# Kernel tuning notes

Measured on AMD Instinct MI355X. Metric: run time of the kernel, lower is better.

Reference implementation:

```python
import jax, jax.numpy as jnp
import numpy as np

IN_DIM, OUT_DIM = 256, 10
N_EXPERTS, N_MEM, STEPS, N_SUB, MAX_K = 12, 32, 6, 5, 5
EXPERT_DIMS = [2048, 2560, 3072, 3584, 4096, 2304, 2816, 3328, 3840, 4608, 3072, 4096]
MAX_E = 4608
N_ITEMS = 4096
SCALE = IN_DIM ** -0.5

def _gelu(x):
    return jax.nn.gelu(x, approximate=False)

_ACTS = [jax.nn.silu, _gelu, lambda x: x * jnp.tanh(jax.nn.softplus(x)), jax.nn.relu,
         jax.nn.selu, jnp.tanh, jax.nn.softplus, jax.nn.elu]
EXPERT_ACTS = [_ACTS[i % 8] for i in range(N_EXPERTS)]

def _ln(x, s, b, eps=1e-5):
    mu = jnp.mean(x, -1, keepdims=True)
    var = jnp.mean((x - mu) ** 2, -1, keepdims=True)
    return (x - mu) * jax.lax.rsqrt(var + eps) * s + b

def _cell(x, ln_s, ln_b, w1, b1, w2, b2):
    h = _gelu(_ln(x, ln_s, ln_b) @ w1.T + b1)
    return x + h @ w2.T + b2

def _ctx_attn(cur, bank, qw, kw, vw):
    # bank: [n, t, d]; single-query dot attention over a small bank
    q = cur @ qw.T
    k = bank @ kw.T
    v = bank @ vw.T
    attn = jax.nn.softmax(jnp.einsum('nd,ntd->nt', q, k) * SCALE, axis=-1)
    return jnp.einsum('nt,ntd->nd', attn, v)

def _renorm_sparse_topk(probs, active_k):
    tv, ti = jax.lax.top_k(probs, MAX_K)
    mask = (jnp.arange(MAX_K)[None, :] < active_k[:, None]).astype(probs.dtype)
    vals = tv * mask
    rows = jnp.arange(probs.shape[0])[:, None]
    sparse = jnp.zeros_like(probs).at[rows, ti].set(vals)
    return sparse / jnp.maximum(jnp.sum(sparse, -1, keepdims=True), 1e-6)

def _fwd(x, W, b,
         shared_up_w, shared_down_w, shared_ln_s, shared_ln_b, shared_scale,
         mem_keys, mem_vals, mem_q_w, mem_out_w, mem_wg_w, mem_wg_b, mem_wv_w, mem_wv_b,
         depth_q_w, depth_k_w, depth_v_w, depth_out_w,
         rc_ln_s, rc_ln_b, rc_w1, rc_b1, rc_w2, rc_b2,
         ssm_in_w, ssm_out_w, ssm_decay,
         sub_w, sub_b, gate_w, gate_b,
         budget_w, budget_b,
         exp_up, exp_down, exp_ln_s, exp_ln_b,
         halt_w, halt_b,
         aux_up_w, aux_down_w, aux_ln_s, aux_ln_b, aux_gate_w, aux_gate_b,
         rf_ln_s, rf_ln_b, rf_w1, rf_b1, rf_w2, rf_b2, reflect_out_w,
         coll_q_w, coll_k_w, coll_v_w, coll_out_w,
         revisit_w, revisit_b,
         vc_ln_s, vc_ln_b, vc_w1, vc_b1, vc_w2, vc_b2,
         ver_q_w, ver_k_w, ver_v_w, ver_out_w, ver_gate_w, ver_gate_b, correction_out_w,
         mix):
    n = x.shape[0]
    base = x @ W.T + b                                                    # [n, out]
    shared = _ln(jax.nn.silu(x @ shared_up_w.T) @ shared_down_w.T, shared_ln_s, shared_ln_b)
    aux = _ln(_gelu(x @ aux_up_w.T) @ aux_down_w.T, aux_ln_s, aux_ln_b)

    mem_vals_b = jnp.broadcast_to(mem_vals[None], (n, N_MEM, IN_DIM))     # per-item memory
    current = x
    mem_logits = jnp.zeros_like(base)
    depth_logits = jnp.zeros_like(base)
    cum_halt = jnp.zeros((n, 1), x.dtype)
    bank = []
    for s in range(STEPS):
        # memory read
        q = current @ mem_q_w.T
        attn = jax.nn.softmax((q @ mem_keys.T) * SCALE, axis=-1)          # [n, slots]
        mem_read = jnp.einsum('ns,nsd->nd', attn, mem_vals_b)
        # gated memory write
        wg = jax.nn.sigmoid(jnp.concatenate([current, mem_read], -1) @ mem_wg_w.T + mem_wg_b)
        wv = current @ mem_wv_w.T + mem_wv_b
        mem_vals_b = mem_vals_b * (1.0 - wg[..., None]) + wg[..., None] * wv[:, None, :]
        # depth attention over previous states
        if bank:
            depth_ctx = _ctx_attn(current, jnp.stack(bank, 1), depth_q_w, depth_k_w, depth_v_w)
        else:
            depth_ctx = jnp.zeros_like(current)
        current = _cell(current + mem_read + depth_ctx,
                        rc_ln_s[s], rc_ln_b[s], rc_w1[s], rc_b1[s], rc_w2[s], rc_b2[s])
        # SSM adapter (single-step gated state update, residual)
        h = jnp.tanh(current @ ssm_in_w.T) * jax.nn.sigmoid(ssm_decay)
        current = current + h @ ssm_out_w.T
        bank.append(current)
        # halting-weighted contributions
        halt = jax.nn.sigmoid((current @ halt_w[s])[:, None] + halt_b[s])
        w_step = (1.0 - cum_halt) * halt
        mem_logits = mem_logits + w_step * (mem_read @ mem_out_w.T)
        depth_logits = depth_logits + w_step * (depth_ctx @ depth_out_w.T)
        cum_halt = jnp.minimum(cum_halt + halt, 1.0)

    # mixture-of-routers + budgeted sparse top-k
    sub_logits = jnp.einsum('nd,sed->nse', current, sub_w) + sub_b        # [n, sub, exp]
    sub_probs = jax.nn.softmax(sub_logits, axis=-1)
    gate = jax.nn.softmax(current @ gate_w.T + gate_b, axis=-1)           # [n, sub]
    probs = jnp.einsum('ns,nse->ne', gate, sub_probs)
    active_k = jnp.argmax(current @ budget_w.T + budget_b, axis=-1) + 1   # 1..MAX_K
    sparse = _renorm_sparse_topk(probs, active_k)                         # [n, exp]

    expert_out = jnp.zeros_like(base)
    for i in range(N_EXPERTS):
        h = EXPERT_ACTS[i](current @ exp_up[i].T)                         # padded to MAX_E
        o = _ln(h @ exp_down[i].T, exp_ln_s[i], exp_ln_b[i])
        expert_out = expert_out + sparse[:, i:i + 1] * o

    # reflection branch
    r = current
    for i in range(3):
        r = _cell(r, rf_ln_s[i], rf_ln_b[i], rf_w1[i], rf_b1[i], rf_w2[i], rf_b2[i])
    reflect_logits = r @ reflect_out_w.T

    # collective attention over state bank + revisit gate
    stack = jnp.stack(bank, 1)
    coll_ctx = _ctx_attn(current, stack, coll_q_w, coll_k_w, coll_v_w)
    coll_logits = coll_ctx @ coll_out_w.T
    revisit = jax.nn.sigmoid(jnp.concatenate([x, current, coll_ctx], -1) @ revisit_w.T + revisit_b)

    # verifier + correction branch
    v = current
    for i in range(2):
        v = _cell(v, vc_ln_s[i], vc_ln_b[i], vc_w1[i], vc_b1[i], vc_w2[i], vc_b2[i])
    ver_ctx = _ctx_attn(v, stack, ver_q_w, ver_k_w, ver_v_w)
    vg = jax.nn.softmax(jnp.concatenate([v, ver_ctx], -1) @ ver_gate_w.T + ver_gate_b, axis=-1)
    ver_logits = ver_ctx @ ver_out_w.T
    corr_logits = v @ correction_out_w.T

    ag = jax.nn.softmax(x @ aux_gate_w.T + aux_gate_b, axis=-1)           # [n, 2]
    alpha, beta, gamma, delta, eps_, zeta = [jnp.tanh(mix[i]) for i in range(6)]
    logits = (base
              + shared_scale * (ag[:, :1] * shared + ag[:, 1:] * aux)
              + alpha * expert_out
              + beta * mem_logits + zeta * depth_logits
              + gamma * reflect_logits
              + delta * revisit * coll_logits
              + eps_ * (vg[:, :1] * ver_logits + vg[:, 1:] * corr_logits))
    return logits


def setup_inputs() -> dict:
    key = jax.random.key(0)
    ks = iter(jax.random.split(key, 128))
    def nrm(shape, std=0.02):
        return jax.random.normal(next(ks), shape, jnp.float32) * std
    d, o = IN_DIM, OUT_DIM
    inp = dict(
        x=jax.random.normal(next(ks), (N_ITEMS, d), jnp.float32),
        W=nrm((o, d), 0.05), b=jnp.zeros((o,), jnp.float32),
        shared_up_w=nrm((3072, d)), shared_down_w=nrm((o, 3072)),
        shared_ln_s=jnp.ones((o,)), shared_ln_b=jnp.zeros((o,)),
        shared_scale=jnp.float32(1.0),
        mem_keys=nrm((N_MEM, d)), mem_vals=nrm((N_MEM, d)),
        mem_q_w=nrm((d, d), 0.01), mem_out_w=nrm((o, d), 0.01),
        mem_wg_w=nrm((N_MEM, 2 * d), 0.01), mem_wg_b=jnp.zeros((N_MEM,)),
        mem_wv_w=nrm((d, d), 0.01), mem_wv_b=jnp.zeros((d,)),
        depth_q_w=nrm((d, d), 0.01), depth_k_w=nrm((d, d), 0.01),
        depth_v_w=nrm((d, d), 0.01), depth_out_w=nrm((o, d), 0.01),
        rc_ln_s=jnp.ones((STEPS, d)), rc_ln_b=jnp.zeros((STEPS, d)),
        rc_w1=nrm((STEPS, 896, d)), rc_b1=jnp.zeros((STEPS, 896)),
        rc_w2=nrm((STEPS, d, 896)), rc_b2=jnp.zeros((STEPS, d)),
        ssm_in_w=nrm((48, d)), ssm_out_w=nrm((d, 48)), ssm_decay=jnp.zeros((48,)),
        sub_w=nrm((N_SUB, N_EXPERTS, d)), sub_b=jnp.zeros((N_SUB, N_EXPERTS)),
        gate_w=nrm((N_SUB, d)), gate_b=jnp.zeros((N_SUB,)),
        budget_w=nrm((MAX_K, d), 0.01), budget_b=jnp.zeros((MAX_K,)),
        halt_w=nrm((STEPS, d), 0.01), halt_b=jnp.full((STEPS,), -2.0, jnp.float32),
        aux_up_w=nrm((4096, d)), aux_down_w=nrm((o, 4096)),
        aux_ln_s=jnp.ones((o,)), aux_ln_b=jnp.zeros((o,)),
        aux_gate_w=nrm((2, d), 0.01), aux_gate_b=jnp.zeros((2,)),
        rf_ln_s=jnp.ones((3, d)), rf_ln_b=jnp.zeros((3, d)),
        rf_w1=nrm((3, 1280, d)), rf_b1=jnp.zeros((3, 1280)),
        rf_w2=nrm((3, d, 1280)), rf_b2=jnp.zeros((3, d)),
        reflect_out_w=nrm((o, d), 0.01),
        coll_q_w=nrm((d, d), 0.01), coll_k_w=nrm((d, d), 0.01),
        coll_v_w=nrm((d, d), 0.01), coll_out_w=nrm((o, d), 0.01),
        revisit_w=nrm((1, 3 * d), 0.01), revisit_b=jnp.zeros((1,)),
        vc_ln_s=jnp.ones((2, d)), vc_ln_b=jnp.zeros((2, d)),
        vc_w1=nrm((2, 1536, d)), vc_b1=jnp.zeros((2, 1536)),
        vc_w2=nrm((2, d, 1536)), vc_b2=jnp.zeros((2, d)),
        ver_q_w=nrm((d, d), 0.01), ver_k_w=nrm((d, d), 0.01),
        ver_v_w=nrm((d, d), 0.01), ver_out_w=nrm((o, d), 0.01),
        ver_gate_w=nrm((2, 2 * d), 0.01), ver_gate_b=jnp.zeros((2,)),
        correction_out_w=nrm((o, d), 0.01),
        mix=jnp.full((6,), 0.5, jnp.float32),
    )
    # variable-width experts padded to MAX_E; padded rows/cols zeroed so math matches
    up = jax.random.normal(next(ks), (N_EXPERTS, MAX_E, d), jnp.float32) * 0.02
    down = jax.random.normal(next(ks), (N_EXPERTS, o, MAX_E), jnp.float32) * 0.01
    col = jnp.arange(MAX_E)
    dims = jnp.array(EXPERT_DIMS)
    mask = (col[None, :] < dims[:, None]).astype(jnp.float32)             # [exp, MAX_E]
    inp['exp_up'] = up * mask[:, :, None]
    inp['exp_down'] = down * mask[:, None, :]
    inp['exp_ln_s'] = jnp.ones((N_EXPERTS, o))
    inp['exp_ln_b'] = jnp.zeros((N_EXPERTS, o))
    return inp


def reference(x, W, b,
              shared_up_w, shared_down_w, shared_ln_s, shared_ln_b, shared_scale,
              mem_keys, mem_vals, mem_q_w, mem_out_w, mem_wg_w, mem_wg_b, mem_wv_w, mem_wv_b,
              depth_q_w, depth_k_w, depth_v_w, depth_out_w,
              rc_ln_s, rc_ln_b, rc_w1, rc_b1, rc_w2, rc_b2,
              ssm_in_w, ssm_out_w, ssm_decay,
              sub_w, sub_b, gate_w, gate_b,
              budget_w, budget_b,
              exp_up, exp_down, exp_ln_s, exp_ln_b,
              halt_w, halt_b,
              aux_up_w, aux_down_w, aux_ln_s, aux_ln_b, aux_gate_w, aux_gate_b,
              rf_ln_s, rf_ln_b, rf_w1, rf_b1, rf_w2, rf_b2, reflect_out_w,
              coll_q_w, coll_k_w, coll_v_w, coll_out_w,
              revisit_w, revisit_b,
              vc_ln_s, vc_ln_b, vc_w1, vc_b1, vc_w2, vc_b2,
              ver_q_w, ver_k_w, ver_v_w, ver_out_w, ver_gate_w, ver_gate_b, correction_out_w,
              mix):
    return _fwd(x, W, b,
                shared_up_w, shared_down_w, shared_ln_s, shared_ln_b, shared_scale,
                mem_keys, mem_vals, mem_q_w, mem_out_w, mem_wg_w, mem_wg_b, mem_wv_w, mem_wv_b,
                depth_q_w, depth_k_w, depth_v_w, depth_out_w,
                rc_ln_s, rc_ln_b, rc_w1, rc_b1, rc_w2, rc_b2,
                ssm_in_w, ssm_out_w, ssm_decay,
                sub_w, sub_b, gate_w, gate_b,
                budget_w, budget_b,
                exp_up, exp_down, exp_ln_s, exp_ln_b,
                halt_w, halt_b,
                aux_up_w, aux_down_w, aux_ln_s, aux_ln_b, aux_gate_w, aux_gate_b,
                rf_ln_s, rf_ln_b, rf_w1, rf_b1, rf_w2, rf_b2, reflect_out_w,
                coll_q_w, coll_k_w, coll_v_w, coll_out_w,
                revisit_w, revisit_b,
                vc_ln_s, vc_ln_b, vc_w1, vc_b1, vc_w2, vc_b2,
                ver_q_w, ver_k_w, ver_v_w, ver_out_w, ver_gate_w, ver_gate_b, correction_out_w,
                mix)
```

## Files before the change

kernel.cpp:

```cpp
#include <hip/hip_runtime.h>


constexpr int NI      = 4096;
constexpr int DIM     = 256;
constexpr int ODIM    = 10;
constexpr int NMEM_   = 32;
constexpr int NSTEPS_ = 6;
constexpr int NEXPERT_= 12;
constexpr int MAXE    = 4608;
#define SCL 0.0625f

__constant__ int EDIMS[NEXPERT_] = {2048,2560,3072,3584,4096,2304,2816,3328,3840,4608,3072,4096};

typedef __attribute__((ext_vector_type(8))) short short8v;
typedef __attribute__((ext_vector_type(4))) float float4v;
typedef __attribute__((ext_vector_type(4))) unsigned short ushort4v;


__device__ __forceinline__ float wred_sum(float v){
  #pragma unroll
  for (int m = 32; m > 0; m >>= 1) v += __shfl_xor(v, m, 64);
  return v;
}
__device__ __forceinline__ float wred_max(float v){
  #pragma unroll
  for (int m = 32; m > 0; m >>= 1) v = fmaxf(v, __shfl_xor(v, m, 64));
  return v;
}
__device__ __forceinline__ float sigm(float x){ return 1.f/(1.f+expf(-x)); }
__device__ __forceinline__ float geluf(float x){ return 0.5f*x*(1.f+erff(x*0.70710678118654752f)); }
__device__ __forceinline__ float softplusf(float x){ return fmaxf(x,0.f) + log1pf(expf(-fabsf(x))); }
__device__ __forceinline__ float act_apply(int a, float x){
  switch(a){
    case 0: return x*sigm(x);
    case 1: return geluf(x);
    case 2: return x*tanhf(softplusf(x));
    case 3: return fmaxf(x,0.f);
    case 4: { const float l=1.0507009873554805f, al=1.6732632423543772f;
              return x>0.f ? l*x : l*al*expm1f(x); }
    case 5: return tanhf(x);
    case 6: return softplusf(x);
    default: return x>0.f ? x : expm1f(x);
  }
}
__device__ __forceinline__ unsigned short f2b(float f){
  unsigned u = __float_as_uint(f);
  u = u + 0x7FFFu + ((u >> 16) & 1u);
  return (unsigned short)(u >> 16);
}
__device__ __forceinline__ void ln10(const float* p, const float* s, const float* b, float* o){
  float mu = 0.f;
  #pragma unroll
  for (int i=0;i<ODIM;i++) mu += p[i];
  mu *= 0.1f;
  float var = 0.f;
  #pragma unroll
  for (int i=0;i<ODIM;i++){ float d = p[i]-mu; var += d*d; }
  var *= 0.1f;
  float rs = 1.f/sqrtf(var + 1e-5f);
  #pragma unroll
  for (int i=0;i<ODIM;i++) o[i] = (p[i]-mu)*rs*s[i] + b[i];
}

__global__ __launch_bounds__(256)
void cvt_k(const float* __restrict__ in, unsigned short* __restrict__ out, int n)
{
  int idx = (blockIdx.x*256 + threadIdx.x)*4;
  if (idx + 3 < n){
    float4 v = *(const float4*)&in[idx];
    ushort4v t; t[0]=f2b(v.x); t[1]=f2b(v.y); t[2]=f2b(v.z); t[3]=f2b(v.w);
    *(ushort4v*)&out[idx] = t;
  }
}

template<int EPI>
__global__ __launch_bounds__(256)
void gemm_k(const float* __restrict__ A, const float* __restrict__ W,
            const float* __restrict__ bias, const float* __restrict__ R,
            const float* __restrict__ vec, float* __restrict__ C,
            int N, int K)
{
  __shared__ float As[32][68];
  __shared__ float Ws[32][68];
  const int bm = blockIdx.y*64, bn = blockIdx.x*64;
  const int tid = threadIdx.x;
  const int tx = tid & 15, ty = tid >> 4;
  const int lrow = tid >> 2, lkq = (tid & 3) * 8;
  float acc[4][4] = {};
  for (int k0 = 0; k0 < K; k0 += 32){
    #pragma unroll
    for (int h = 0; h < 2; ++h){
      int kk = lkq + h*4;
      float4 va = make_float4(0.f,0.f,0.f,0.f), vw = make_float4(0.f,0.f,0.f,0.f);
      if (k0 + kk < K)
        va = *(const float4*)&A[(size_t)(bm+lrow)*K + k0 + kk];
      if (bn + lrow < N && k0 + kk < K)
        vw = *(const float4*)&W[(size_t)(bn+lrow)*K + k0 + kk];
      As[kk+0][lrow]=va.x; As[kk+1][lrow]=va.y; As[kk+2][lrow]=va.z; As[kk+3][lrow]=va.w;
      Ws[kk+0][lrow]=vw.x; Ws[kk+1][lrow]=vw.y; Ws[kk+2][lrow]=vw.z; Ws[kk+3][lrow]=vw.w;
    }
    __syncthreads();
    #pragma unroll
    for (int kk = 0; kk < 32; ++kk){
      float4 a4 = *(const float4*)&As[kk][ty*4];
      float4 b4 = *(const float4*)&Ws[kk][tx*4];
      float av[4] = {a4.x,a4.y,a4.z,a4.w};
      float bv[4] = {b4.x,b4.y,b4.z,b4.w};
      #pragma unroll
      for (int i=0;i<4;i++)
        #pragma unroll
        for (int j=0;j<4;j++) acc[i][j] = fmaf(av[i], bv[j], acc[i][j]);
    }
    __syncthreads();
  }
  #pragma unroll
  for (int i=0;i<4;i++){
    int r = bm + ty*4 + i;
    #pragma unroll
    for (int j=0;j<4;j++){
      int c = bn + tx*4 + j;
      if (c >= N) continue;
      float v = acc[i][j];
      if constexpr (EPI==1) v += bias[c];
      else if constexpr (EPI==2) v = geluf(v + bias[c]);
      else if constexpr (EPI==3) v = v + bias[c] + R[(size_t)r*N + c];
      else if constexpr (EPI==4) v = tanhf(v) * sigm(vec[c]);
      else if constexpr (EPI==5) v = v + R[(size_t)r*N + c];
      C[(size_t)r*N + c] = v;
    }
  }
}

template<int EPI>
__global__ __launch_bounds__(256)
void bgemm_k(const short* __restrict__ A, const short* __restrict__ B,
             const float* __restrict__ bias, const float* __restrict__ R,
             float* __restrict__ Cf, unsigned short* __restrict__ Cb,
             int N, int K)
{
  __shared__ short As[128][40];
  __shared__ short Bsm[64][40];
  const int bm = blockIdx.y*128, bn = blockIdx.x*64;
  const int tid = threadIdx.x;
  const int wave = tid >> 6, lane = tid & 63;
  const int l15 = lane & 15, lg = lane >> 4;
  const int ar = tid >> 1, ah = tid & 1;
  float4v acc[2][4] = {};
  for (int k0 = 0; k0 < K; k0 += 32){
    __syncthreads();
    { const short* src = A + (size_t)(bm+ar)*K + k0 + ah*16;
      short8v v0 = *(const short8v*)src;
      short8v v1 = *(const short8v*)(src+8);
      *(short8v*)&As[ar][ah*16]   = v0;
      *(short8v*)&As[ar][ah*16+8] = v1; }
    if (tid < 128){
      const short* src = B + (size_t)(bn+ar)*K + k0 + ah*16;
      short8v v0 = *(const short8v*)src;
      short8v v1 = *(const short8v*)(src+8);
      *(short8v*)&Bsm[ar][ah*16]   = v0;
      *(short8v*)&Bsm[ar][ah*16+8] = v1; }
    __syncthreads();
    short8v bfr[4];
    #pragma unroll
    for (int nt = 0; nt < 4; nt++)
      bfr[nt] = *(const short8v*)&Bsm[nt*16 + l15][lg*8];
    #pragma unroll
    for (int mt = 0; mt < 2; mt++){
      short8v a = *(const short8v*)&As[wave*32 + mt*16 + l15][lg*8];
      #pragma unroll
      for (int nt = 0; nt < 4; nt++)
        acc[mt][nt] = __builtin_amdgcn_mfma_f32_16x16x32_bf16(a, bfr[nt], acc[mt][nt], 0, 0, 0);
    }
  }
  #pragma unroll
  for (int mt = 0; mt < 2; mt++)
    #pragma unroll
    for (int nt = 0; nt < 4; nt++)
      #pragma unroll
      for (int reg = 0; reg < 4; reg++){
        int row = bm + wave*32 + mt*16 + lg*4 + reg;
        int col = bn + nt*16 + l15;
        float v = acc[mt][nt][reg];
        if constexpr (EPI==0){
          v = geluf(v + bias[col]);
          Cb[(size_t)row*N + col] = f2b(v);
        } else {
          v = v + bias[col] + R[(size_t)row*N + col];
          Cf[(size_t)row*N + col] = v;
        }
      }
}

__global__ __launch_bounds__(512)
void moe_k(const float* __restrict__ cur, const float* __restrict__ x,
           const float* __restrict__ exp_up, const float* __restrict__ shared_up,
           const float* __restrict__ aux_up, const short* __restrict__ upb,
           const float* __restrict__ exp_down, const float* __restrict__ shared_down,
           const float* __restrict__ aux_down,
           float* __restrict__ expert_pre, float* __restrict__ shared_pre,
           float* __restrict__ aux_pre)
{
  __shared__ short Bs[64][264];
  __shared__ float Ds[64][12];
  const int z = blockIdx.y;
  const int bm = blockIdx.x * 128;
  const int tid = threadIdx.x;
  const int wave = tid >> 6, lane = tid & 63;
  const int l15 = lane & 15, lg = lane >> 4;

  int E, act, dstride;
  const float* upf; const short* upbz; const float* down; float* outp;
  if (z < NEXPERT_){
    E = EDIMS[z]; act = z & 7;
    upf = exp_up + (size_t)z*MAXE*DIM;
    upbz = upb ? upb + (size_t)z*MAXE*DIM : nullptr;
    down = exp_down + (size_t)z*ODIM*MAXE; dstride = MAXE;
    outp = expert_pre + (size_t)z*NI*ODIM;
  } else if (z == NEXPERT_){
    E = 3072; act = 0; upf = shared_up;
    upbz = upb ? upb + (size_t)NEXPERT_*MAXE*DIM : nullptr;
    down = shared_down; dstride = 3072; outp = shared_pre;
  } else {
    E = 4096; act = 1; upf = aux_up;
    upbz = upb ? upb + (size_t)NEXPERT_*MAXE*DIM + (size_t)3072*DIM : nullptr;
    down = aux_down; dstride = 4096; outp = aux_pre;
  }
  const float* X = (z < NEXPERT_) ? cur : x;

  short8v afrag[8];
  {
    const float* xr = X + (size_t)(bm + wave*16 + l15)*DIM;
    #pragma unroll
    for (int ks = 0; ks < 8; ks++){
      float4 v0 = *(const float4*)&xr[ks*32 + lg*8];
      float4 v1 = *(const float4*)&xr[ks*32 + lg*8 + 4];
      short8v a;
      a[0]=(short)f2b(v0.x); a[1]=(short)f2b(v0.y); a[2]=(short)f2b(v0.z); a[3]=(short)f2b(v0.w);
      a[4]=(short)f2b(v1.x); a[5]=(short)f2b(v1.y); a[6]=(short)f2b(v1.z); a[7]=(short)f2b(v1.w);
      afrag[ks] = a;
    }
  }
  float racc[4][10];
  #pragma unroll
  for (int r = 0; r < 4; r++)
    #pragma unroll
    for (int o = 0; o < 10; o++) racc[r][o] = 0.f;

  const int sr = tid >> 3, sp = tid & 7;
  for (int c = 0; c < E; c += 64){
    __syncthreads();
    if (upbz){
      const short* src = upbz + (size_t)(c + sr)*DIM + sp*32;
      short8v v0 = *(const short8v*)(src);
      short8v v1 = *(const short8v*)(src+8);
      short8v v2 = *(const short8v*)(src+16);
      short8v v3 = *(const short8v*)(src+24);
      *(short8v*)&Bs[sr][sp*32]    = v0;
      *(short8v*)&Bs[sr][sp*32+8]  = v1;
      *(short8v*)&Bs[sr][sp*32+16] = v2;
      *(short8v*)&Bs[sr][sp*32+24] = v3;
    } else {
      const float* src = upf + (size_t)(c + sr)*DIM + sp*32;
      #pragma unroll
      for (int seg = 0; seg < 4; seg++){
        float4 f0 = *(const float4*)&src[seg*8];
        float4 f1 = *(const float4*)&src[seg*8+4];
        short8v s;
        s[0]=(short)f2b(f0.x); s[1]=(short)f2b(f0.y); s[2]=(short)f2b(f0.z); s[3]=(short)f2b(f0.w);
        s[4]=(short)f2b(f1.x); s[5]=(short)f2b(f1.y); s[6]=(short)f2b(f1.z); s[7]=(short)f2b(f1.w);
        *(short8v*)&Bs[sr][sp*32+seg*8] = s;
      }
    }
    for (int t2 = tid; t2 < 640; t2 += 512){
      int e = t2 & 63, o = t2 >> 6;
      Ds[e][o] = down[(size_t)o*dstride + c + e];
    }
    __syncthreads();

    float4v acc[4] = {};
    #pragma unroll
    for (int ks = 0; ks < 8; ks++){
      #pragma unroll
      for (int nt = 0; nt < 4; nt++){
        short8v b = *(const short8v*)&Bs[nt*16 + l15][ks*32 + lg*8];
        acc[nt] = __builtin_amdgcn_mfma_f32_16x16x32_bf16(afrag[ks], b, acc[nt], 0, 0, 0);
      }
    }
    #pragma unroll
    for (int nt = 0; nt < 4; nt++){
      const float* dp = &Ds[nt*16 + l15][0];
      float4 d0 = *(const float4*)dp;
      float4 d1 = *(const float4*)(dp+4);
      float  d8 = dp[8], d9 = dp[9];
      float dv[10] = {d0.x,d0.y,d0.z,d0.w,d1.x,d1.y,d1.z,d1.w,d8,d9};
      float hv[4];
      #pragma unroll
      for (int reg = 0; reg < 4; reg++) hv[reg] = act_apply(act, acc[nt][reg]);
      #pragma unroll
      for (int o = 0; o < 10; o++)
        #pragma unroll
        for (int reg = 0; reg < 4; reg++)
          racc[reg][o] = fmaf(hv[reg], dv[o], racc[reg][o]);
    }
  }
  #pragma unroll
  for (int reg = 0; reg < 4; reg++)
    #pragma unroll
    for (int o = 0; o < 10; o++){
      float v = racc[reg][o];
      v += __shfl_xor(v, 1, 64); v += __shfl_xor(v, 2, 64);
      v += __shfl_xor(v, 4, 64); v += __shfl_xor(v, 8, 64);
      racc[reg][o] = v;
    }
  if (l15 == 0){
    #pragma unroll
    for (int reg = 0; reg < 4; reg++){
      int row = bm + wave*16 + lg*4 + reg;
      #pragma unroll
      for (int o = 0; o < 10; o++)
        outp[(size_t)row*ODIM + o] = racc[reg][o];
    }
  }
}

__global__ __launch_bounds__(256)
void thin_k(const float* __restrict__ A1, int K1,
            const float* __restrict__ A2, int K2,
            const float* __restrict__ W, const float* __restrict__ bias,
            float* __restrict__ C, int NO, int post)
{
  int idx = blockIdx.x*256 + threadIdx.x;
  if (idx >= NI*NO) return;
  int item = idx / NO, o = idx - item*NO;
  const float* w = W + (size_t)o*(K1+K2);
  const float* a1 = A1 + (size_t)item*K1;
  float s = 0.f;
  for (int k = 0; k < K1; k += 4){
    float4 av = *(const float4*)&a1[k];
    float4 wv = *(const float4*)&w[k];
    s = fmaf(av.x,wv.x, fmaf(av.y,wv.y, fmaf(av.z,wv.z, fmaf(av.w,wv.w, s))));
  }
  if (A2){
    const float* a2 = A2 + (size_t)item*K2;
    const float* w2 = w + K1;
    for (int k = 0; k < K2; k += 4){
      float4 av = *(const float4*)&a2[k];
      float4 wv = *(const float4*)&w2[k];
      s = fmaf(av.x,wv.x, fmaf(av.y,wv.y, fmaf(av.z,wv.z, fmaf(av.w,wv.w, s))));
    }
  }
  if (bias) s += bias[o];
  if (post == 1) s = sigm(s);
  else if (post == 2) s *= SCL;
  C[(size_t)item*NO + o] = s;
}

__global__ void atb_k(const float* __restrict__ A, const float* __restrict__ B,
                      float* __restrict__ C, int M, int I, int J)
{
  int idx = blockIdx.x*256 + threadIdx.x;
  if (idx >= I*J) return;
  int i = idx / J, j = idx - i*J;
  float s = 0.f;
  for (int m = 0; m < M; m++) s = fmaf(A[(size_t)m*I+i], B[(size_t)m*J+j], s);
  C[idx] = s;
}
__global__ void ab_k(const float* __restrict__ A, const float* __restrict__ B,
                     float* __restrict__ C, int M, int K, int N)
{
  int idx = blockIdx.x*256 + threadIdx.x;
  if (idx >= M*N) return;
  int i = idx / N, j = idx - i*N;
  float s = 0.f;
  for (int k = 0; k < K; k++) s = fmaf(A[(size_t)i*K+k], B[(size_t)k*N+j], s);
  C[idx] = s;
}

__global__ __launch_bounds__(256)
void ln3_k(const float* __restrict__ a, const float* __restrict__ b,
           const float* __restrict__ c, const float* __restrict__ lns,
           const float* __restrict__ lnb, float* __restrict__ xout,
           float* __restrict__ lnout, unsigned short* __restrict__ lnout_b)
{
  int item = blockIdx.x*4 + (threadIdx.x >> 6);
  int lane = threadIdx.x & 63;
  float4 v = ((const float4*)(a + (size_t)item*DIM))[lane];
  if (b){ float4 t = ((const float4*)(b + (size_t)item*DIM))[lane]; v.x+=t.x; v.y+=t.y; v.z+=t.z; v.w+=t.w; }
  if (c){ float4 t = ((const float4*)(c + (size_t)item*DIM))[lane]; v.x+=t.x; v.y+=t.y; v.z+=t.z; v.w+=t.w; }
  if (xout) ((float4*)(xout + (size_t)item*DIM))[lane] = v;
  float mu = wred_sum(v.x+v.y+v.z+v.w) * (1.f/DIM);
  float dx=v.x-mu, dy=v.y-mu, dz=v.z-mu, dw=v.w-mu;
  float var = wred_sum(dx*dx+dy*dy+dz*dz+dw*dw) * (1.f/DIM);
  float rs = 1.f/sqrtf(var + 1e-5f);
  float4 s4 = ((const float4*)lns)[lane];
  float4 b4 = ((const float4*)lnb)[lane];
  float4 o4 = make_float4(dx*rs*s4.x + b4.x, dy*rs*s4.y + b4.y,
                          dz*rs*s4.z + b4.z, dw*rs*s4.w + b4.w);
  if (lnout) ((float4*)(lnout + (size_t)item*DIM))[lane] = o4;
  if (lnout_b){
    ushort4v t; t[0]=f2b(o4.x); t[1]=f2b(o4.y); t[2]=f2b(o4.z); t[3]=f2b(o4.w);
    *(ushort4v*)(lnout_b + (size_t)item*DIM + lane*4) = t;
  }
}

__global__ __launch_bounds__(256)
void memread_k(const float* __restrict__ sc, const float* __restrict__ a_state,
               const float* __restrict__ c_state, const float* __restrict__ mem_vals,
               const float* __restrict__ wv_hist, float* __restrict__ mem_read, int step)
{
  int item = blockIdx.x*4 + (threadIdx.x >> 6);
  int lane = threadIdx.x & 63;
  float v = (lane < NMEM_) ? sc[(size_t)item*NMEM_ + lane] : -1e30f;
  float m = wred_max(v);
  float e = (lane < NMEM_) ? expf(v - m) : 0.f;
  float inv = 1.f / wred_sum(e);
  float attn = e * inv;
  float aval = 0.f;
  if (lane < NMEM_) aval = (step == 0) ? 1.f : a_state[(size_t)item*NMEM_ + lane];
  float wslot = attn * aval;
  float beta[NSTEPS_];
  #pragma unroll
  for (int t = 0; t < NSTEPS_; t++){
    beta[t] = 0.f;
    if (t < step){
      float cc = (lane < NMEM_) ? c_state[((size_t)item*NMEM_ + lane)*NSTEPS_ + t] : 0.f;
      beta[t] = wred_sum(attn * cc);
    }
  }
  float ax=0.f, ay=0.f, az=0.f, aw=0.f;
  #pragma unroll
  for (int s2 = 0; s2 < NMEM_; s2++){
    float ws = __shfl(wslot, s2, 64);
    float4 mv = ((const float4*)(mem_vals + (size_t)s2*DIM))[lane];
    ax = fmaf(ws, mv.x, ax); ay = fmaf(ws, mv.y, ay);
    az = fmaf(ws, mv.z, az); aw = fmaf(ws, mv.w, aw);
  }
  #pragma unroll
  for (int t = 0; t < NSTEPS_; t++){
    if (t < step){
      float4 h4 = ((const float4*)(wv_hist + ((size_t)t*NI + item)*DIM))[lane];
      ax = fmaf(beta[t], h4.x, ax); ay = fmaf(beta[t], h4.y, ay);
      az = fmaf(beta[t], h4.z, az); aw = fmaf(beta[t], h4.w, aw);
    }
  }
  ((float4*)(mem_read + (size_t)item*DIM))[lane] = make_float4(ax,ay,az,aw);
}

__global__ void state_k(const float* __restrict__ wg, float* __restrict__ a_state,
                        float* __restrict__ c_state, int step)
{
  int idx = blockIdx.x*256 + threadIdx.x;
  if (idx >= NI*NMEM_) return;
  float g = wg[idx];
  float om = 1.f - g;
  float a = (step == 0) ? 1.f : a_state[idx];
  a_state[idx] = a * om;
  float* c = c_state + (size_t)idx*NSTEPS_;
  #pragma unroll
  for (int t = 0; t < NSTEPS_; t++) if (t < step) c[t] *= om;
  c[step] = g;
}

__global__ __launch_bounds__(256)
void bankattn_k(const float* __restrict__ q2, const float* __restrict__ bank,
                float* __restrict__ wsum, int t)
{
  int item = blockIdx.x*4 + (threadIdx.x >> 6);
  int lane = threadIdx.x & 63;
  float4 q4 = ((const float4*)(q2 + (size_t)item*DIM))[lane];
  float sc[NSTEPS_];
  float4 bb[NSTEPS_];
  #pragma unroll
  for (int j = 0; j < NSTEPS_; j++){
    if (j < t){
      bb[j] = ((const float4*)(bank + ((size_t)j*NI + item)*DIM))[lane];
      sc[j] = wred_sum(q4.x*bb[j].x + q4.y*bb[j].y + q4.z*bb[j].z + q4.w*bb[j].w) * SCL;
    }
  }
  float mx = -1e30f;
  #pragma unroll
  for (int j = 0; j < NSTEPS_; j++) if (j < t) mx = fmaxf(mx, sc[j]);
  float se = 0.f;
  #pragma unroll
  for (int j = 0; j < NSTEPS_; j++) if (j < t){ sc[j] = expf(sc[j]-mx); se += sc[j]; }
  float inv = 1.f/se;
  float ax=0.f, ay=0.f, az=0.f, aw=0.f;
  #pragma unroll
  for (int j = 0; j < NSTEPS_; j++){
    if (j < t){
      float a = sc[j]*inv;
      ax = fmaf(a, bb[j].x, ax); ay = fmaf(a, bb[j].y, ay);
      az = fmaf(a, bb[j].z, az); aw = fmaf(a, bb[j].w, aw);
    }
  }
  ((float4*)(wsum + (size_t)item*DIM))[lane] = make_float4(ax,ay,az,aw);
}

__global__ __launch_bounds__(256)
void halt_k(const float* __restrict__ cur, const float* __restrict__ mem_read,
            const float* __restrict__ depth_ctx, const float* __restrict__ halt_w,
            const float* __restrict__ halt_b, const float* __restrict__ mem_out_w,
            const float* __restrict__ depth_out_w, float* __restrict__ mem_logits,
            float* __restrict__ depth_logits, float* __restrict__ cum_halt, int step)
{
  int item = blockIdx.x*4 + (threadIdx.x >> 6);
  int lane = threadIdx.x & 63;
  float4 c4 = ((const float4*)(cur + (size_t)item*DIM))[lane];
  float4 hw = ((const float4*)(halt_w + (size_t)step*DIM))[lane];
  float hd = wred_sum(c4.x*hw.x + c4.y*hw.y + c4.z*hw.z + c4.w*hw.w);
  float halt = sigm(hd + halt_b[step]);
  float ch = cum_halt[item];
  float wstep = (1.f - ch) * halt;
  float4 m4 = ((const float4*)(mem_read + (size_t)item*DIM))[lane];
  float4 d4 = make_float4(0.f,0.f,0.f,0.f);
  if (step > 0) d4 = ((const float4*)(depth_ctx + (size_t)item*DIM))[lane];
  #pragma unroll
  for (int o = 0; o < ODIM; o++){
    float4 w4 = ((const float4*)(mem_out_w + (size_t)o*DIM))[lane];
    float s = wred_sum(m4.x*w4.x + m4.y*w4.y + m4.z*w4.z + m4.w*w4.w);
    if (lane == 0) mem_logits[(size_t)item*ODIM + o] += wstep * s;
    if (step > 0){
      float4 v4 = ((const float4*)(depth_out_w + (size_t)o*DIM))[lane];
      float s2 = wred_sum(d4.x*v4.x + d4.y*v4.y + d4.z*v4.z + d4.w*v4.w);
      if (lane == 0) depth_logits[(size_t)item*ODIM + o] += wstep * s2;
    }
  }
  if (lane == 0) cum_halt[item] = fminf(ch + halt, 1.f);
}

__global__ void router_k(const float* __restrict__ sub60, const float* __restrict__ gate5,
                         const float* __restrict__ budget5, float* __restrict__ sparse)
{
  int item = blockIdx.x*256 + threadIdx.x;
  if (item >= NI) return;
  float probs[NEXPERT_];
  #pragma unroll
  for (int e = 0; e < NEXPERT_; e++) probs[e] = 0.f;
  float g[5];
  float gm = -1e30f;
  #pragma unroll
  for (int s = 0; s < 5; s++){ g[s] = gate5[(size_t)item*5 + s]; gm = fmaxf(gm, g[s]); }
  float gs = 0.f;
  #pragma unroll
  for (int s = 0; s < 5; s++){ g[s] = expf(g[s]-gm); gs += g[s]; }
  float gi = 1.f/gs;
  #pragma unroll
  for (int s = 0; s < 5; s++){
    float sl[NEXPERT_];
    float mx = -1e30f;
    #pragma unroll
    for (int e = 0; e < NEXPERT_; e++){ sl[e] = sub60[(size_t)item*60 + s*NEXPERT_ + e]; mx = fmaxf(mx, sl[e]); }
    float se = 0.f;
    #pragma unroll
    for (int e = 0; e < NEXPERT_; e++){ sl[e] = expf(sl[e]-mx); se += sl[e]; }
    float w = g[s]*gi/se;
    #pragma unroll
    for (int e = 0; e < NEXPERT_; e++) probs[e] = fmaf(w, sl[e], probs[e]);
  }
  float bl0 = budget5[(size_t)item*5];
  int am = 0;
  #pragma unroll
  for (int s = 1; s < 5; s++){ float bv = budget5[(size_t)item*5 + s]; if (bv > bl0){ bl0 = bv; am = s; } }
  int kact = am + 1;
  unsigned used = 0;
  float tv[5]; int ti[5];
  float ssum = 0.f;
  #pragma unroll
  for (int j = 0; j < 5; j++){
    float bv = -1e30f; int bi = 0;
    #pragma unroll
    for (int e = 0; e < NEXPERT_; e++){
      bool ok = !((used >> e) & 1u);
      if (ok && probs[e] > bv){ bv = probs[e]; bi = e; }
    }
    used |= (1u << bi);
    tv[j] = bv; ti[j] = bi;
    if (j < kact) ssum += bv;
  }
  float den = 1.f/fmaxf(ssum, 1e-6f);
  #pragma unroll
  for (int e = 0; e < NEXPERT_; e++){
    float v = 0.f;
    #pragma unroll
    for (int j = 0; j < 5; j++) if (j < kact && ti[j] == e) v = tv[j];
    sparse[(size_t)item*NEXPERT_ + e] = v*den;
  }
}

__global__ void final_k(
  const float* __restrict__ x, const float* __restrict__ cur,
  const float* __restrict__ vbuf, const float* __restrict__ coll_ctx,
  const float* __restrict__ ver_ctx,
  const float* __restrict__ base10, const float* __restrict__ shared_pre,
  const float* __restrict__ aux_pre, const float* __restrict__ expert_pre,
  const float* __restrict__ sparse, const float* __restrict__ mem_logits,
  const float* __restrict__ depth_logits, const float* __restrict__ reflect10,
  const float* __restrict__ coll10, const float* __restrict__ ver10,
  const float* __restrict__ corr10,
  const float* __restrict__ shared_ln_s, const float* __restrict__ shared_ln_b,
  const float* __restrict__ aux_ln_s, const float* __restrict__ aux_ln_b,
  const float* __restrict__ exp_ln_s, const float* __restrict__ exp_ln_b,
  const float* __restrict__ aux_gate_w, const float* __restrict__ aux_gate_b,
  const float* __restrict__ ver_gate_w, const float* __restrict__ ver_gate_b,
  const float* __restrict__ revisit_w, const float* __restrict__ revisit_b,
  const float* __restrict__ shared_scale, const float* __restrict__ mix,
  float* __restrict__ out)
{
  int item = blockIdx.x*256 + threadIdx.x;
  if (item >= NI) return;
  const float* xr = x + (size_t)item*DIM;
  const float* cr = cur + (size_t)item*DIM;
  const float* vr = vbuf + (size_t)item*DIM;
  const float* lr = coll_ctx + (size_t)item*DIM;
  const float* tr = ver_ctx + (size_t)item*DIM;
  float ag0 = aux_gate_b[0], ag1 = aux_gate_b[1];
  for (int k = 0; k < DIM; k++){
    float xv = xr[k];
    ag0 = fmaf(xv, aux_gate_w[k], ag0);
    ag1 = fmaf(xv, aux_gate_w[DIM+k], ag1);
  }
  { float m = fmaxf(ag0,ag1); float e0 = expf(ag0-m), e1 = expf(ag1-m);
    float i2 = 1.f/(e0+e1); ag0 = e0*i2; ag1 = e1*i2; }
  float vg0 = ver_gate_b[0], vg1 = ver_gate_b[1];
  for (int k = 0; k < DIM; k++){
    vg0 = fmaf(vr[k], ver_gate_w[k], vg0);
    vg1 = fmaf(vr[k], ver_gate_w[512+k], vg1);
  }
  for (int k = 0; k < DIM; k++){
    vg0 = fmaf(tr[k], ver_gate_w[DIM+k], vg0);
    vg1 = fmaf(tr[k], ver_gate_w[512+DIM+k], vg1);
  }
  { float m = fmaxf(vg0,vg1); float e0 = expf(vg0-m), e1 = expf(vg1-m);
    float i2 = 1.f/(e0+e1); vg0 = e0*i2; vg1 = e1*i2; }
  float rv = revisit_b[0];
  for (int k = 0; k < DIM; k++){
    rv = fmaf(xr[k], revisit_w[k], rv);
    rv = fmaf(cr[k], revisit_w[DIM+k], rv);
    rv = fmaf(lr[k], revisit_w[2*DIM+k], rv);
  }
  rv = sigm(rv);
  float sh[ODIM], axl[ODIM];
  { float tmp[ODIM];
    #pragma unroll
    for (int o = 0; o < ODIM; o++) tmp[o] = shared_pre[(size_t)item*ODIM + o];
    ln10(tmp, shared_ln_s, shared_ln_b, sh);
    #pragma unroll
    for (int o = 0; o < ODIM; o++) tmp[o] = aux_pre[(size_t)item*ODIM + o];
    ln10(tmp, aux_ln_s, aux_ln_b, axl); }
  float eo[ODIM];
  #pragma unroll
  for (int o = 0; o < ODIM; o++) eo[o] = 0.f;
  for (int i2 = 0; i2 < NEXPERT_; i2++){
    float sp = sparse[(size_t)item*NEXPERT_ + i2];
    if (sp != 0.f){
      float tmp[ODIM], lo[ODIM];
      #pragma unroll
      for (int o = 0; o < ODIM; o++) tmp[o] = expert_pre[((size_t)i2*NI + item)*ODIM + o];
      ln10(tmp, exp_ln_s + i2*ODIM, exp_ln_b + i2*ODIM, lo);
      #pragma unroll
      for (int o = 0; o < ODIM; o++) eo[o] = fmaf(sp, lo[o], eo[o]);
    }
  }
  float al = tanhf(mix[0]), be = tanhf(mix[1]), ga = tanhf(mix[2]);
  float de = tanhf(mix[3]), ep = tanhf(mix[4]), ze = tanhf(mix[5]);
  float ss = shared_scale[0];
  #pragma unroll
  for (int o = 0; o < ODIM; o++){
    size_t ix = (size_t)item*ODIM + o;
    float v = base10[ix]
      + ss*(ag0*sh[o] + ag1*axl[o])
      + al*eo[o]
      + be*mem_logits[ix] + ze*depth_logits[ix]
      + ga*reflect10[ix]
      + de*rv*coll10[ix]
      + ep*(vg0*ver10[ix] + vg1*corr10[ix]);
    out[ix] = v;
  }
}


static void launch_gemm(int epi, const float* A, const float* W, const float* b,
                        const float* R, const float* vec, float* C, int N, int K,
                        hipStream_t stream)
{
  dim3 g((N+63)/64, NI/64), blk(256);
  switch(epi){
    case 0: gemm_k<0><<<g,blk,0,stream>>>(A,W,b,R,vec,C,N,K); break;
    case 1: gemm_k<1><<<g,blk,0,stream>>>(A,W,b,R,vec,C,N,K); break;
    case 2: gemm_k<2><<<g,blk,0,stream>>>(A,W,b,R,vec,C,N,K); break;
    case 3: gemm_k<3><<<g,blk,0,stream>>>(A,W,b,R,vec,C,N,K); break;
    case 4: gemm_k<4><<<g,blk,0,stream>>>(A,W,b,R,vec,C,N,K); break;
    case 5: gemm_k<5><<<g,blk,0,stream>>>(A,W,b,R,vec,C,N,K); break;
  }
}

static void launch_cvt(const float* in, unsigned short* out, size_t n, hipStream_t stream)
{
  cvt_k<<<(unsigned)((n/4 + 255)/256), 256, 0, stream>>>(in, out, (int)n);
}

extern "C" void kernel_launch(void* const* d_in, const int* in_sizes, int n_in,
                              void* d_out, int out_size, void* d_ws, size_t ws_size,
                              hipStream_t stream)
{
  (void)in_sizes; (void)n_in; (void)out_size;
  const float* x             = (const float*)d_in[0];
  const float* Wm            = (const float*)d_in[1];
  const float* bvec          = (const float*)d_in[2];
  const float* shared_up_w   = (const float*)d_in[3];
  const float* shared_down_w = (const float*)d_in[4];
  const float* shared_ln_s   = (const float*)d_in[5];
  const float* shared_ln_b   = (const float*)d_in[6];
  const float* shared_scale  = (const float*)d_in[7];
  const float* mem_keys      = (const float*)d_in[8];
  const float* mem_vals      = (const float*)d_in[9];
  const float* mem_q_w       = (const float*)d_in[10];
  const float* mem_out_w     = (const float*)d_in[11];
  const float* mem_wg_w      = (const float*)d_in[12];
  const float* mem_wg_b      = (const float*)d_in[13];
  const float* mem_wv_w      = (const float*)d_in[14];
  const float* mem_wv_b      = (const float*)d_in[15];
  const float* depth_q_w     = (const float*)d_in[16];
  const float* depth_k_w     = (const float*)d_in[17];
  const float* depth_v_w     = (const float*)d_in[18];
  const float* depth_out_w   = (const float*)d_in[19];
  const float* rc_ln_s       = (const float*)d_in[20];
  const float* rc_ln_b       = (const float*)d_in[21];
  const float* rc_w1         = (const float*)d_in[22];
  const float* rc_b1         = (const float*)d_in[23];
  const float* rc_w2         = (const float*)d_in[24];
  const float* rc_b2         = (const float*)d_in[25];
  const float* ssm_in_w      = (const float*)d_in[26];
  const float* ssm_out_w     = (const float*)d_in[27];
  const float* ssm_decay     = (const float*)d_in[28];
  const float* sub_w         = (const float*)d_in[29];
  const float* sub_b         = (const float*)d_in[30];
  const float* gate_w        = (const float*)d_in[31];
  const float* gate_b        = (const float*)d_in[32];
  const float* budget_w      = (const float*)d_in[33];
  const float* budget_b      = (const float*)d_in[34];
  const float* halt_w        = (const float*)d_in[35];
  const float* halt_b        = (const float*)d_in[36];
  const float* aux_up_w      = (const float*)d_in[37];
  const float* aux_down_w    = (const float*)d_in[38];
  const float* aux_ln_s      = (const float*)d_in[39];
  const float* aux_ln_b      = (const float*)d_in[40];
  const float* aux_gate_w    = (const float*)d_in[41];
  const float* aux_gate_b    = (const float*)d_in[42];
  const float* rf_ln_s       = (const float*)d_in[43];
  const float* rf_ln_b       = (const float*)d_in[44];
  const float* rf_w1         = (const float*)d_in[45];
  const float* rf_b1         = (const float*)d_in[46];
  const float* rf_w2         = (const float*)d_in[47];
  const float* rf_b2         = (const float*)d_in[48];
  const float* reflect_out_w = (const float*)d_in[49];
  const float* coll_q_w      = (const float*)d_in[50];
  const float* coll_k_w      = (const float*)d_in[51];
  const float* coll_v_w      = (const float*)d_in[52];
  const float* coll_out_w    = (const float*)d_in[53];
  const float* revisit_w     = (const float*)d_in[54];
  const float* revisit_b     = (const float*)d_in[55];
  const float* vc_ln_s       = (const float*)d_in[56];
  const float* vc_ln_b       = (const float*)d_in[57];
  const float* vc_w1         = (const float*)d_in[58];
  const float* vc_b1         = (const float*)d_in[59];
  const float* vc_w2         = (const float*)d_in[60];
  const float* vc_b2         = (const float*)d_in[61];
  const float* ver_q_w       = (const float*)d_in[62];
  const float* ver_k_w       = (const float*)d_in[63];
  const float* ver_v_w       = (const float*)d_in[64];
  const float* ver_out_w     = (const float*)d_in[65];
  const float* ver_gate_w    = (const float*)d_in[66];
  const float* ver_gate_b    = (const float*)d_in[67];
  const float* correction_out_w = (const float*)d_in[68];
  const float* mix           = (const float*)d_in[69];
  const float* exp_up        = (const float*)d_in[70];
  const float* exp_down      = (const float*)d_in[71];
  const float* exp_ln_s      = (const float*)d_in[72];
  const float* exp_ln_b      = (const float*)d_in[73];
  float* out = (float*)d_out;

  float* w = (float*)d_ws;
  size_t off = 0;
  auto WS = [&](size_t nf){ float* p = w + off; off += nf; return p; };
  float* bank      = WS((size_t)NSTEPS_*NI*DIM);
  float* cur_in    = WS((size_t)NI*DIM);
  float* t_ln      = WS((size_t)NI*DIM);
  float* hbig      = WS((size_t)NI*896);
  float* mem_read  = WS((size_t)NI*DIM);
  float* depth_ctx = WS((size_t)NI*DIM);
  float* q2        = WS((size_t)NI*DIM);
  float* wsumb     = WS((size_t)NI*DIM);
  float* wv_hist   = WS((size_t)NSTEPS_*NI*DIM);
  float* wg        = WS((size_t)NI*NMEM_);
  float* mem_sc    = WS((size_t)NI*NMEM_);
  float* a_state   = WS((size_t)NI*NMEM_);
  float* c_state   = WS((size_t)NI*NMEM_*NSTEPS_);
  float* h48       = WS((size_t)NI*48);
  float* rbuf      = WS((size_t)NI*DIM);
  float* vbuf      = WS((size_t)NI*DIM);
  float* coll_ctx  = WS((size_t)NI*DIM);
  float* ver_ctx   = WS((size_t)NI*DIM);
  float* sub60     = WS((size_t)NI*60);
  float* gate5     = WS((size_t)NI*5);
  float* budget5   = WS((size_t)NI*5);
  float* sparse    = WS((size_t)NI*NEXPERT_);
  float* base10    = WS((size_t)NI*ODIM);
  float* reflect10 = WS((size_t)NI*ODIM);
  float* coll10    = WS((size_t)NI*ODIM);
  float* ver10     = WS((size_t)NI*ODIM);
  float* corr10    = WS((size_t)NI*ODIM);
  float* PdT       = WS((size_t)DIM*DIM);
  float* PcT       = WS((size_t)DIM*DIM);
  float* PvT       = WS((size_t)DIM*DIM);
  float* MK        = WS((size_t)NMEM_*DIM);
  float* zbase     = w + off;
  float* mem_logits   = WS((size_t)NI*ODIM);
  float* depth_logits = WS((size_t)NI*ODIM);
  float* shared_pre   = WS((size_t)NI*ODIM);
  float* aux_pre      = WS((size_t)NI*ODIM);
  float* expert_pre   = WS((size_t)NEXPERT_*NI*ODIM);
  float* cum_halt     = WS((size_t)NI);
  size_t zbytes = (size_t)((w + off) - zbase) * sizeof(float);
  hipMemsetAsync((void*)zbase, 0, zbytes, stream);

  unsigned short* bb = (unsigned short*)(w + off);
  size_t boff = 0;
  auto BS = [&](size_t ns){ unsigned short* p = bb + boff; boff += ns; return p; };
  unsigned short* t_ln_b = BS((size_t)NI*DIM);
  unsigned short* rfw1b  = BS((size_t)3*1280*DIM);
  unsigned short* rfw2b  = BS((size_t)3*DIM*1280);
  unsigned short* vcw1b  = BS((size_t)2*1536*DIM);
  unsigned short* vcw2b  = BS((size_t)2*DIM*1536);
  unsigned short* upb    = bb + boff;
  size_t upb_n = ((size_t)NEXPERT_*MAXE + 3072 + 4096) * DIM;
  size_t base_bytes = off*sizeof(float) + boff*sizeof(unsigned short);
  bool use_upb = (ws_size >= base_bytes + upb_n*sizeof(unsigned short));
  unsigned short* hb = (unsigned short*)hbig;

  auto thin = [&](const float* A1, int K1, const float* A2, int K2,
                  const float* Wp, const float* bp, float* Cp, int NO, int post){
    int total = NI*NO;
    thin_k<<<(total+255)/256, 256, 0, stream>>>(A1,K1,A2,K2,Wp,bp,Cp,NO,post);
  };

  launch_cvt(rf_w1, rfw1b, (size_t)3*1280*DIM, stream);
  launch_cvt(rf_w2, rfw2b, (size_t)3*DIM*1280, stream);
  launch_cvt(vc_w1, vcw1b, (size_t)2*1536*DIM, stream);
  launch_cvt(vc_w2, vcw2b, (size_t)2*DIM*1536, stream);
  if (use_upb){
    launch_cvt(exp_up,      upb,                                    (size_t)NEXPERT_*MAXE*DIM, stream);
    launch_cvt(shared_up_w, upb + (size_t)NEXPERT_*MAXE*DIM,        (size_t)3072*DIM, stream);
    launch_cvt(aux_up_w,    upb + (size_t)NEXPERT_*MAXE*DIM + (size_t)3072*DIM, (size_t)4096*DIM, stream);
  }

  atb_k<<<(DIM*DIM+255)/256, 256, 0, stream>>>(depth_k_w, depth_q_w, PdT, DIM, DIM, DIM);
  atb_k<<<(DIM*DIM+255)/256, 256, 0, stream>>>(coll_k_w,  coll_q_w,  PcT, DIM, DIM, DIM);
  atb_k<<<(DIM*DIM+255)/256, 256, 0, stream>>>(ver_k_w,   ver_q_w,   PvT, DIM, DIM, DIM);
  ab_k <<<(NMEM_*DIM+255)/256, 256, 0, stream>>>(mem_keys, mem_q_w, MK, NMEM_, DIM, DIM);

  thin(x, DIM, nullptr, 0, Wm, bvec, base10, ODIM, 0);

  const float* cur = x;
  for (int s = 0; s < NSTEPS_; s++){
    thin(cur, DIM, nullptr, 0, MK, nullptr, mem_sc, NMEM_, 2);
    memread_k<<<NI/4, 256, 0, stream>>>(mem_sc, a_state, c_state, mem_vals, wv_hist, mem_read, s);
    thin(cur, DIM, mem_read, DIM, mem_wg_w, mem_wg_b, wg, NMEM_, 1);
    launch_gemm(1, cur, mem_wv_w, mem_wv_b, nullptr, nullptr,
                wv_hist + (size_t)s*NI*DIM, DIM, DIM, stream);
    state_k<<<(NI*NMEM_+255)/256, 256, 0, stream>>>(wg, a_state, c_state, s);
    if (s > 0){
      launch_gemm(0, cur, PdT, nullptr, nullptr, nullptr, q2, DIM, DIM, stream);
      bankattn_k<<<NI/4, 256, 0, stream>>>(q2, bank, wsumb, s);
      launch_gemm(0, wsumb, depth_v_w, nullptr, nullptr, nullptr, depth_ctx, DIM, DIM, stream);
    }
    ln3_k<<<NI/4, 256, 0, stream>>>(cur, mem_read, (s > 0 ? depth_ctx : nullptr),
                                    rc_ln_s + (size_t)s*DIM, rc_ln_b + (size_t)s*DIM,
                                    cur_in, t_ln, nullptr);
    launch_gemm(2, t_ln, rc_w1 + (size_t)s*896*DIM, rc_b1 + (size_t)s*896,
                nullptr, nullptr, hbig, 896, DIM, stream);
    launch_gemm(3, hbig, rc_w2 + (size_t)s*DIM*896, rc_b2 + (size_t)s*DIM,
                cur_in, nullptr, cur_in, DIM, 896, stream);
    launch_gemm(4, cur_in, ssm_in_w, nullptr, nullptr, ssm_decay, h48, 48, DIM, stream);
    float* newcur = bank + (size_t)s*NI*DIM;
    launch_gemm(5, h48, ssm_out_w, nullptr, cur_in, nullptr, newcur, DIM, 48, stream);
    halt_k<<<NI/4, 256, 0, stream>>>(newcur, mem_read, depth_ctx, halt_w, halt_b,
                                     mem_out_w, depth_out_w, mem_logits, depth_logits,
                                     cum_halt, s);
    cur = newcur;
  }

  thin(cur, DIM, nullptr, 0, sub_w, sub_b, sub60, 60, 0);
  thin(cur, DIM, nullptr, 0, gate_w, gate_b, gate5, 5, 0);
  thin(cur, DIM, nullptr, 0, budget_w, budget_b, budget5, 5, 0);
  router_k<<<(NI+255)/256, 256, 0, stream>>>(sub60, gate5, budget5, sparse);

  moe_k<<<dim3(NI/128, NEXPERT_+2), 512, 0, stream>>>(
      cur, x, exp_up, shared_up_w, aux_up_w, use_upb ? (const short*)upb : nullptr,
      exp_down, shared_down_w, aux_down_w, expert_pre, shared_pre, aux_pre);

  const float* rsrc = cur;
  for (int i = 0; i < 3; i++){
    ln3_k<<<NI/4, 256, 0, stream>>>(rsrc, nullptr, nullptr,
                                    rf_ln_s + (size_t)i*DIM, rf_ln_b + (size_t)i*DIM,
                                    nullptr, nullptr, t_ln_b);
    bgemm_k<0><<<dim3(1280/64, NI/128), 256, 0, stream>>>(
        (const short*)t_ln_b, (const short*)(rfw1b + (size_t)i*1280*DIM),
        rf_b1 + (size_t)i*1280, nullptr, nullptr, hb, 1280, DIM);
    bgemm_k<1><<<dim3(DIM/64, NI/128), 256, 0, stream>>>(
        (const short*)hb, (const short*)(rfw2b + (size_t)i*DIM*1280),
        rf_b2 + (size_t)i*DIM, rsrc, rbuf, nullptr, DIM, 1280);
    rsrc = rbuf;
  }

  const float* vsrc = cur;
  for (int i = 0; i < 2; i++){
    ln3_k<<<NI/4, 256, 0, stream>>>(vsrc, nullptr, nullptr,
                                    vc_ln_s + (size_t)i*DIM, vc_ln_b + (size_t)i*DIM,
                                    nullptr, nullptr, t_ln_b);
    bgemm_k<0><<<dim3(1536/64, NI/128), 256, 0, stream>>>(
        (const short*)t_ln_b, (const short*)(vcw1b + (size_t)i*1536*DIM),
        vc_b1 + (size_t)i*1536, nullptr, nullptr, hb, 1536, DIM);
    bgemm_k<1><<<dim3(DIM/64, NI/128), 256, 0, stream>>>(
        (const short*)hb, (const short*)(vcw2b + (size_t)i*DIM*1536),
        vc_b2 + (size_t)i*DIM, vsrc, vbuf, nullptr, DIM, 1536);
    vsrc = vbuf;
  }

  launch_gemm(0, cur, PcT, nullptr, nullptr, nullptr, q2, DIM, DIM, stream);
  bankattn_k<<<NI/4, 256, 0, stream>>>(q2, bank, wsumb, NSTEPS_);
  launch_gemm(0, wsumb, coll_v_w, nullptr, nullptr, nullptr, coll_ctx, DIM, DIM, stream);

  launch_gemm(0, vbuf, PvT, nullptr, nullptr, nullptr, q2, DIM, DIM, stream);
  bankattn_k<<<NI/4, 256, 0, stream>>>(q2, bank, wsumb, NSTEPS_);
  launch_gemm(0, wsumb, ver_v_w, nullptr, nullptr, nullptr, ver_ctx, DIM, DIM, stream);

  thin(rbuf,     DIM, nullptr, 0, reflect_out_w,    nullptr, reflect10, ODIM, 0);
  thin(coll_ctx, DIM, nullptr, 0, coll_out_w,       nullptr, coll10,    ODIM, 0);
  thin(ver_ctx,  DIM, nullptr, 0, ver_out_w,        nullptr, ver10,     ODIM, 0);
  thin(vbuf,     DIM, nullptr, 0, correction_out_w, nullptr, corr10,    ODIM, 0);

  final_k<<<(NI+255)/256, 256, 0, stream>>>(
      x, cur, vbuf, coll_ctx, ver_ctx,
      base10, shared_pre, aux_pre, expert_pre, sparse,
      mem_logits, depth_logits, reflect10, coll10, ver10, corr10,
      shared_ln_s, shared_ln_b, aux_ln_s, aux_ln_b, exp_ln_s, exp_ln_b,
      aux_gate_w, aux_gate_b, ver_gate_w, ver_gate_b, revisit_w, revisit_b,
      shared_scale, mix, out);
}
```

Before: 3.044 ms.

## Split MoE over expert column chunks and fuse thin projections into consumers

The MoE kernel is re-gridded so each block handles a 256-column slice of one expert, with prepacked, LDS-swizzled bf16 up-weights and atomicAdd accumulation of the down projection, which spreads uneven expert sizes across many more blocks. The small projections are folded into the kernels that consume them: memory scores into memread, gate writes into a fused memwrite, the SSM into the halt kernel, router logits into the router, and the output heads into one kernel. This removes many launches and intermediate buffers. The atomics make the MoE output depend on zero-initialised buffers and on a nondeterministic summation order.

```diff
diff --git a/kernel.cpp b/kernel.cpp
--- a/kernel.cpp
+++ b/kernel.cpp
@@ -8,9 +8,13 @@
 constexpr int NSTEPS_ = 6;
 constexpr int NEXPERT_= 12;
 constexpr int MAXE    = 4608;
+constexpr int TOTCOL  = 46592;
 #define SCL 0.0625f
 
-__constant__ int EDIMS[NEXPERT_] = {2048,2560,3072,3584,4096,2304,2816,3328,3840,4608,3072,4096};
+__constant__ int GCNT[14] = {8,10,12,14,16,9,11,13,15,18,12,16,12,16};
+__constant__ int CCNT[14] = {32,40,48,56,64,36,44,52,60,72,48,64,48,64};
+__constant__ int ZCOL[14] = {0,2048,4608,7680,11264,15360,17664,20480,
+                             23808,27648,32256,35328,39424,42496};
 
 typedef __attribute__((ext_vector_type(8))) short short8v;
 typedef __attribute__((ext_vector_type(4))) float float4v;
@@ -48,6 +52,15 @@
   u = u + 0x7FFFu + ((u >> 16) & 1u);
   return (unsigned short)(u >> 16);
 }
+__device__ __forceinline__ float dot256f(const float* __restrict__ a,
+                                         const float* __restrict__ w, float s){
+  for (int k = 0; k < DIM; k += 4){
+    float4 av = *(const float4*)&a[k];
+    float4 wv = *(const float4*)&w[k];
+    s = fmaf(av.x,wv.x, fmaf(av.y,wv.y, fmaf(av.z,wv.z, fmaf(av.w,wv.w, s))));
+  }
+  return s;
+}
 __device__ __forceinline__ void ln10(const float* p, const float* s, const float* b, float* o){
   float mu = 0.f;
   #pragma unroll
@@ -73,12 +86,39 @@
   }
 }
 
+__global__ __launch_bounds__(512)
+void cvtup_k(const float* __restrict__ exp_up, const float* __restrict__ shared_up,
+             const float* __restrict__ aux_up, short* __restrict__ upb)
+{
+  int chunk = blockIdx.x;
+  int z = 0, crem = chunk;
+  while (crem >= CCNT[z]){ crem -= CCNT[z]; z++; }
+  const float* src;
+  if (z < 12)       src = exp_up + (size_t)z*MAXE*DIM;
+  else if (z == 12) src = shared_up;
+  else              src = aux_up;
+  int colbase = crem*64;
+  short* dst = upb + (size_t)chunk*16384;
+  int t = threadIdx.x;
+  int c = t >> 3, kb = (t & 7)*32;
+  const float* srow = src + (size_t)(colbase + c)*DIM + kb;
+  #pragma unroll
+  for (int j = 0; j < 4; j++){
+    float4 f0 = *(const float4*)&srow[j*8];
+    float4 f1 = *(const float4*)&srow[j*8+4];
+    short8v s;
+    s[0]=(short)f2b(f0.x); s[1]=(short)f2b(f0.y); s[2]=(short)f2b(f0.z); s[3]=(short)f2b(f0.w);
+    s[4]=(short)f2b(f1.x); s[5]=(short)f2b(f1.y); s[6]=(short)f2b(f1.z); s[7]=(short)f2b(f1.w);
+    int kq = (t & 7)*4 + j;
+    *(short8v*)&dst[((size_t)kq*64 + c)*8] = s;
+  }
+}
+
 template<int EPI>
 __global__ __launch_bounds__(256)
 void gemm_k(const float* __restrict__ A, const float* __restrict__ W,
             const float* __restrict__ bias, const float* __restrict__ R,
-            const float* __restrict__ vec, float* __restrict__ C,
-            int N, int K)
+            float* __restrict__ C, int N, int K)
 {
   __shared__ float As[32][68];
   __shared__ float Ws[32][68];
@@ -124,8 +164,6 @@
       if constexpr (EPI==1) v += bias[c];
       else if constexpr (EPI==2) v = geluf(v + bias[c]);
       else if constexpr (EPI==3) v = v + bias[c] + R[(size_t)r*N + c];
-      else if constexpr (EPI==4) v = tanhf(v) * sigm(vec[c]);
-      else if constexpr (EPI==5) v = v + R[(size_t)r*N + c];
       C[(size_t)r*N + c] = v;
     }
   }
@@ -192,40 +230,34 @@
 }
 
 __global__ __launch_bounds__(512)
-void moe_k(const float* __restrict__ cur, const float* __restrict__ x,
-           const float* __restrict__ exp_up, const float* __restrict__ shared_up,
-           const float* __restrict__ aux_up, const short* __restrict__ upb,
-           const float* __restrict__ exp_down, const float* __restrict__ shared_down,
-           const float* __restrict__ aux_down,
-           float* __restrict__ expert_pre, float* __restrict__ shared_pre,
-           float* __restrict__ aux_pre)
-{
-  __shared__ short Bs[64][264];
+void moe2_k(const float* __restrict__ cur, const float* __restrict__ x,
+            const float* __restrict__ exp_up, const float* __restrict__ shared_up,
+            const float* __restrict__ aux_up, const short* __restrict__ upb,
+            const float* __restrict__ exp_down, const float* __restrict__ shared_down,
+            const float* __restrict__ aux_down,
+            float* __restrict__ expert_pre, float* __restrict__ shared_pre,
+            float* __restrict__ aux_pre)
+{
+  __shared__ short Bs[16384];
   __shared__ float Ds[64][12];
-  const int z = blockIdx.y;
-  const int bm = blockIdx.x * 128;
-  const int tid = threadIdx.x;
-  const int wave = tid >> 6, lane = tid & 63;
-  const int l15 = lane & 15, lg = lane >> 4;
-
-  int E, act, dstride;
-  const float* upf; const short* upbz; const float* down; float* outp;
+  int gy = blockIdx.y, z = 0;
+  while (gy >= GCNT[z]){ gy -= GCNT[z]; z++; }
+  const int localcol = gy*256;
+  int act, dstride; const float* upf; const float* down; float* outp;
   if (z < NEXPERT_){
-    E = EDIMS[z]; act = z & 7;
+    act = z & 7;
     upf = exp_up + (size_t)z*MAXE*DIM;
-    upbz = upb ? upb + (size_t)z*MAXE*DIM : nullptr;
     down = exp_down + (size_t)z*ODIM*MAXE; dstride = MAXE;
     outp = expert_pre + (size_t)z*NI*ODIM;
   } else if (z == NEXPERT_){
-    E = 3072; act = 0; upf = shared_up;
-    upbz = upb ? upb + (size_t)NEXPERT_*MAXE*DIM : nullptr;
-    down = shared_down; dstride = 3072; outp = shared_pre;
+    act = 0; upf = shared_up; down = shared_down; dstride = 3072; outp = shared_pre;
   } else {
-    E = 4096; act = 1; upf = aux_up;
-    upbz = upb ? upb + (size_t)NEXPERT_*MAXE*DIM + (size_t)3072*DIM : nullptr;
-    down = aux_down; dstride = 4096; outp = aux_pre;
+    act = 1; upf = aux_up; down = aux_down; dstride = 4096; outp = aux_pre;
   }
   const float* X = (z < NEXPERT_) ? cur : x;
+  const int bm = blockIdx.x*128;
+  const int tid = threadIdx.x, wave = tid >> 6, lane = tid & 63;
+  const int l15 = lane & 15, lg = lane >> 4;
 
   short8v afrag[8];
   {
@@ -246,34 +278,38 @@
     #pragma unroll
     for (int o = 0; o < 10; o++) racc[r][o] = 0.f;
 
-  const int sr = tid >> 3, sp = tid & 7;
-  for (int c = 0; c < E; c += 64){
+  const int sc = tid & 63, sw = tid >> 6;
+  const int gchunk0 = (ZCOL[z] + localcol) >> 6;
+  for (int ch = 0; ch < 4; ch++){
+    const int cb = localcol + ch*64;
     __syncthreads();
-    if (upbz){
-      const short* src = upbz + (size_t)(c + sr)*DIM + sp*32;
-      short8v v0 = *(const short8v*)(src);
-      short8v v1 = *(const short8v*)(src+8);
-      short8v v2 = *(const short8v*)(src+16);
-      short8v v3 = *(const short8v*)(src+24);
-      *(short8v*)&Bs[sr][sp*32]    = v0;
-      *(short8v*)&Bs[sr][sp*32+8]  = v1;
-      *(short8v*)&Bs[sr][sp*32+16] = v2;
-      *(short8v*)&Bs[sr][sp*32+24] = v3;
+    if (upb){
+      const short* chunk = upb + ((size_t)(gchunk0 + ch))*16384;
+      #pragma unroll
+      for (int i = 0; i < 4; i++){
+        int u = tid + 512*i;
+        short8v v = *(const short8v*)&chunk[(size_t)u*8];
+        int c = u & 63, kq = u >> 6;
+        int byteoff = ((c << 9) + (kq << 4)) ^ ((c & 7) << 4);
+        *(short8v*)((char*)Bs + byteoff) = v;
+      }
     } else {
-      const float* src = upf + (size_t)(c + sr)*DIM + sp*32;
+      const float* srow = upf + (size_t)(cb + sc)*DIM;
       #pragma unroll
-      for (int seg = 0; seg < 4; seg++){
-        float4 f0 = *(const float4*)&src[seg*8];
-        float4 f1 = *(const float4*)&src[seg*8+4];
+      for (int i = 0; i < 4; i++){
+        int kq = sw + 8*i;
+        float4 f0 = *(const float4*)&srow[kq*8];
+        float4 f1 = *(const float4*)&srow[kq*8 + 4];
         short8v s;
         s[0]=(short)f2b(f0.x); s[1]=(short)f2b(f0.y); s[2]=(short)f2b(f0.z); s[3]=(short)f2b(f0.w);
         s[4]=(short)f2b(f1.x); s[5]=(short)f2b(f1.y); s[6]=(short)f2b(f1.z); s[7]=(short)f2b(f1.w);
-        *(short8v*)&Bs[sr][sp*32+seg*8] = s;
+        int byteoff = ((sc << 9) + (kq << 4)) ^ ((sc & 7) << 4);
+        *(short8v*)((char*)Bs + byteoff) = s;
       }
     }
     for (int t2 = tid; t2 < 640; t2 += 512){
       int e = t2 & 63, o = t2 >> 6;
-      Ds[e][o] = down[(size_t)o*dstride + c + e];
+      Ds[e][o] = down[(size_t)o*dstride + cb + e];
     }
     __syncthreads();
 
@@ -282,7 +318,9 @@
     for (int ks = 0; ks < 8; ks++){
       #pragma unroll
       for (int nt = 0; nt < 4; nt++){
-        short8v b = *(const short8v*)&Bs[nt*16 + l15][ks*32 + lg*8];
+        int c = nt*16 + l15, kq = ks*4 + lg;
+        int byteoff = ((c << 9) + (kq << 4)) ^ ((c & 7) << 4);
+        short8v b = *(const short8v*)((const char*)Bs + byteoff);
         acc[nt] = __builtin_amdgcn_mfma_f32_16x16x32_bf16(afrag[ks], b, acc[nt], 0, 0, 0);
       }
     }
@@ -290,7 +328,7 @@
     for (int nt = 0; nt < 4; nt++){
       const float* dp = &Ds[nt*16 + l15][0];
       float4 d0 = *(const float4*)dp;
-      float4 d1 = *(const float4*)(dp+4);
+      float4 d1 = *(const float4*)(dp + 4);
       float  d8 = dp[8], d9 = dp[9];
       float dv[10] = {d0.x,d0.y,d0.z,d0.w,d1.x,d1.y,d1.z,d1.w,d8,d9};
       float hv[4];
@@ -318,41 +356,9 @@
       int row = bm + wave*16 + lg*4 + reg;
       #pragma unroll
       for (int o = 0; o < 10; o++)
-        outp[(size_t)row*ODIM + o] = racc[reg][o];
-    }
-  }
-}
-
-__global__ __launch_bounds__(256)
-void thin_k(const float* __restrict__ A1, int K1,
-            const float* __restrict__ A2, int K2,
-            const float* __restrict__ W, const float* __restrict__ bias,
-            float* __restrict__ C, int NO, int post)
-{
-  int idx = blockIdx.x*256 + threadIdx.x;
-  if (idx >= NI*NO) return;
-  int item = idx / NO, o = idx - item*NO;
-  const float* w = W + (size_t)o*(K1+K2);
-  const float* a1 = A1 + (size_t)item*K1;
-  float s = 0.f;
-  for (int k = 0; k < K1; k += 4){
-    float4 av = *(const float4*)&a1[k];
-    float4 wv = *(const float4*)&w[k];
-    s = fmaf(av.x,wv.x, fmaf(av.y,wv.y, fmaf(av.z,wv.z, fmaf(av.w,wv.w, s))));
-  }
-  if (A2){
-    const float* a2 = A2 + (size_t)item*K2;
-    const float* w2 = w + K1;
-    for (int k = 0; k < K2; k += 4){
-      float4 av = *(const float4*)&a2[k];
-      float4 wv = *(const float4*)&w2[k];
-      s = fmaf(av.x,wv.x, fmaf(av.y,wv.y, fmaf(av.z,wv.z, fmaf(av.w,wv.w, s))));
-    }
-  }
-  if (bias) s += bias[o];
-  if (post == 1) s = sigm(s);
-  else if (post == 2) s *= SCL;
-  C[(size_t)item*NO + o] = s;
+        atomicAdd(&outp[(size_t)row*ODIM + o], racc[reg][o]);
+    }
+  }
 }
 
 __global__ void atb_k(const float* __restrict__ A, const float* __restrict__ B,
@@ -404,13 +410,16 @@
 }
 
 __global__ __launch_bounds__(256)
-void memread_k(const float* __restrict__ sc, const float* __restrict__ a_state,
-               const float* __restrict__ c_state, const float* __restrict__ mem_vals,
-               const float* __restrict__ wv_hist, float* __restrict__ mem_read, int step)
+void memread2_k(const float* __restrict__ cur, const float* __restrict__ MK,
+                const float* __restrict__ a_state, const float* __restrict__ c_state,
+                const float* __restrict__ mem_vals, const float* __restrict__ wv_hist,
+                float* __restrict__ mem_read, int step)
 {
   int item = blockIdx.x*4 + (threadIdx.x >> 6);
   int lane = threadIdx.x & 63;
-  float v = (lane < NMEM_) ? sc[(size_t)item*NMEM_ + lane] : -1e30f;
+  float v = -1e30f;
+  if (lane < NMEM_)
+    v = dot256f(cur + (size_t)item*DIM, MK + (size_t)lane*DIM, 0.f) * SCL;
   float m = wred_max(v);
   float e = (lane < NMEM_) ? expf(v - m) : 0.f;
   float inv = 1.f / wred_sum(e);
@@ -446,12 +455,20 @@
   ((float4*)(mem_read + (size_t)item*DIM))[lane] = make_float4(ax,ay,az,aw);
 }
 
-__global__ void state_k(const float* __restrict__ wg, float* __restrict__ a_state,
-                        float* __restrict__ c_state, int step)
-{
-  int idx = blockIdx.x*256 + threadIdx.x;
-  if (idx >= NI*NMEM_) return;
-  float g = wg[idx];
+__global__ __launch_bounds__(256)
+void memwrite_k(const float* __restrict__ cur, const float* __restrict__ mem_read,
+                const float* __restrict__ mem_wg_w, const float* __restrict__ mem_wg_b,
+                float* __restrict__ a_state, float* __restrict__ c_state, int step)
+{
+  int item = blockIdx.x*4 + (threadIdx.x >> 6);
+  int lane = threadIdx.x & 63;
+  if (lane >= NMEM_) return;
+  const float* wr = mem_wg_w + (size_t)lane*2*DIM;
+  float s = dot256f(cur + (size_t)item*DIM, wr, 0.f);
+  s = dot256f(mem_read + (size_t)item*DIM, wr + DIM, s);
+  s += mem_wg_b[lane];
+  float g = sigm(s);
+  int idx = item*NMEM_ + lane;
   float om = 1.f - g;
   float a = (step == 0) ? 1.f : a_state[idx];
   a_state[idx] = a * om;
@@ -497,17 +514,39 @@
 }
 
 __global__ __launch_bounds__(256)
-void halt_k(const float* __restrict__ cur, const float* __restrict__ mem_read,
-            const float* __restrict__ depth_ctx, const float* __restrict__ halt_w,
-            const float* __restrict__ halt_b, const float* __restrict__ mem_out_w,
-            const float* __restrict__ depth_out_w, float* __restrict__ mem_logits,
-            float* __restrict__ depth_logits, float* __restrict__ cum_halt, int step)
-{
-  int item = blockIdx.x*4 + (threadIdx.x >> 6);
+void ssmhalt_k(const float* __restrict__ cur_in, const float* __restrict__ mem_read,
+               const float* __restrict__ depth_ctx,
+               const float* __restrict__ ssm_in_w, const float* __restrict__ ssm_out_w,
+               const float* __restrict__ ssm_decay,
+               const float* __restrict__ halt_w, const float* __restrict__ halt_b,
+               const float* __restrict__ mem_out_w, const float* __restrict__ depth_out_w,
+               float* __restrict__ newcur, float* __restrict__ mem_logits,
+               float* __restrict__ depth_logits, float* __restrict__ cum_halt, int step)
+{
+  __shared__ float sh48[4][48];
+  int wi = threadIdx.x >> 6;
+  int item = blockIdx.x*4 + wi;
   int lane = threadIdx.x & 63;
-  float4 c4 = ((const float4*)(cur + (size_t)item*DIM))[lane];
+  const float* ci = cur_in + (size_t)item*DIM;
+  if (lane < 48){
+    float s = dot256f(ci, ssm_in_w + (size_t)lane*DIM, 0.f);
+    sh48[wi][lane] = tanhf(s) * sigm(ssm_decay[lane]);
+  }
+  __syncthreads();
+  float4 nc = ((const float4*)ci)[lane];
+  float o0 = nc.x, o1 = nc.y, o2 = nc.z, o3 = nc.w;
+  const float* so = ssm_out_w + (size_t)(lane*4)*48;
+  #pragma unroll 8
+  for (int j = 0; j < 48; j++){
+    float h = sh48[wi][j];
+    o0 = fmaf(h, so[j],       o0);
+    o1 = fmaf(h, so[48 + j],  o1);
+    o2 = fmaf(h, so[96 + j],  o2);
+    o3 = fmaf(h, so[144 + j], o3);
+  }
+  ((float4*)(newcur + (size_t)item*DIM))[lane] = make_float4(o0,o1,o2,o3);
   float4 hw = ((const float4*)(halt_w + (size_t)step*DIM))[lane];
-  float hd = wred_sum(c4.x*hw.x + c4.y*hw.y + c4.z*hw.z + c4.w*hw.w);
+  float hd = wred_sum(o0*hw.x + o1*hw.y + o2*hw.z + o3*hw.w);
   float halt = sigm(hd + halt_b[step]);
   float ch = cum_halt[item];
   float wstep = (1.f - ch) * halt;
@@ -528,18 +567,33 @@
   if (lane == 0) cum_halt[item] = fminf(ch + halt, 1.f);
 }
 
-__global__ void router_k(const float* __restrict__ sub60, const float* __restrict__ gate5,
-                         const float* __restrict__ budget5, float* __restrict__ sparse)
-{
-  int item = blockIdx.x*256 + threadIdx.x;
-  if (item >= NI) return;
+__global__ __launch_bounds__(256)
+void router2_k(const float* __restrict__ cur,
+               const float* __restrict__ sub_w, const float* __restrict__ sub_b,
+               const float* __restrict__ gate_w, const float* __restrict__ gate_b,
+               const float* __restrict__ budget_w, const float* __restrict__ budget_b,
+               float* __restrict__ sparse)
+{
+  __shared__ float S[4][72];
+  int wi = threadIdx.x >> 6;
+  int item = blockIdx.x*4 + wi;
+  int lane = threadIdx.x & 63;
+  const float* cr = cur + (size_t)item*DIM;
+  if (lane < 60)
+    S[wi][lane] = dot256f(cr, sub_w + (size_t)lane*DIM, 0.f) + sub_b[lane];
+  if (lane < 5)
+    S[wi][60 + lane] = dot256f(cr, gate_w + (size_t)lane*DIM, 0.f) + gate_b[lane];
+  else if (lane >= 32 && lane < 37)
+    S[wi][65 + lane - 32] = dot256f(cr, budget_w + (size_t)(lane-32)*DIM, 0.f) + budget_b[lane-32];
+  __syncthreads();
+  if (lane != 0) return;
   float probs[NEXPERT_];
   #pragma unroll
   for (int e = 0; e < NEXPERT_; e++) probs[e] = 0.f;
   float g[5];
   float gm = -1e30f;
   #pragma unroll
-  for (int s = 0; s < 5; s++){ g[s] = gate5[(size_t)item*5 + s]; gm = fmaxf(gm, g[s]); }
+  for (int s = 0; s < 5; s++){ g[s] = S[wi][60+s]; gm = fmaxf(gm, g[s]); }
   float gs = 0.f;
   #pragma unroll
   for (int s = 0; s < 5; s++){ g[s] = expf(g[s]-gm); gs += g[s]; }
@@ -549,7 +603,7 @@
     float sl[NEXPERT_];
     float mx = -1e30f;
     #pragma unroll
-    for (int e = 0; e < NEXPERT_; e++){ sl[e] = sub60[(size_t)item*60 + s*NEXPERT_ + e]; mx = fmaxf(mx, sl[e]); }
+    for (int e = 0; e < NEXPERT_; e++){ sl[e] = S[wi][s*NEXPERT_ + e]; mx = fmaxf(mx, sl[e]); }
     float se = 0.f;
     #pragma unroll
     for (int e = 0; e < NEXPERT_; e++){ sl[e] = expf(sl[e]-mx); se += sl[e]; }
@@ -557,10 +611,10 @@
     #pragma unroll
     for (int e = 0; e < NEXPERT_; e++) probs[e] = fmaf(w, sl[e], probs[e]);
   }
-  float bl0 = budget5[(size_t)item*5];
+  float bl0 = S[wi][65];
   int am = 0;
   #pragma unroll
-  for (int s = 1; s < 5; s++){ float bv = budget5[(size_t)item*5 + s]; if (bv > bl0){ bl0 = bv; am = s; } }
+  for (int s = 1; s < 5; s++){ float bv = S[wi][65+s]; if (bv > bl0){ bl0 = bv; am = s; } }
   int kact = am + 1;
   unsigned used = 0;
   float tv[5]; int ti[5];
@@ -585,6 +639,31 @@
     for (int j = 0; j < 5; j++) if (j < kact && ti[j] == e) v = tv[j];
     sparse[(size_t)item*NEXPERT_ + e] = v*den;
   }
+}
+
+__global__ __launch_bounds__(256)
+void heads_k(const float* __restrict__ rbuf, const float* __restrict__ coll_ctx,
+             const float* __restrict__ ver_ctx, const float* __restrict__ vbuf,
+             const float* __restrict__ x,
+             const float* __restrict__ reflect_out_w, const float* __restrict__ coll_out_w,
+             const float* __restrict__ ver_out_w, const float* __restrict__ correction_out_w,
+             const float* __restrict__ Wm, const float* __restrict__ bvec,
+             float* __restrict__ reflect10, float* __restrict__ coll10,
+             float* __restrict__ ver10, float* __restrict__ corr10,
+             float* __restrict__ base10)
+{
+  int idx = blockIdx.x*256 + threadIdx.x;
+  if (idx >= NI*50) return;
+  int which = idx / (NI*ODIM), rem = idx - which*NI*ODIM;
+  int item = rem / ODIM, o = rem - item*ODIM;
+  const float* A; const float* Wp; float* C; float b2 = 0.f;
+  if      (which == 0){ A = rbuf;     Wp = reflect_out_w;    C = reflect10; }
+  else if (which == 1){ A = coll_ctx; Wp = coll_out_w;       C = coll10; }
+  else if (which == 2){ A = ver_ctx;  Wp = ver_out_w;        C = ver10; }
+  else if (which == 3){ A = vbuf;     Wp = correction_out_w; C = corr10; }
+  else               { A = x;        Wp = Wm;               C = base10; b2 = bvec[o]; }
+  float s = dot256f(A + (size_t)item*DIM, Wp + (size_t)o*DIM, 0.f) + b2;
+  C[(size_t)item*ODIM + o] = s;
 }
 
 __global__ void final_k(
@@ -680,17 +759,14 @@
 
 
 static void launch_gemm(int epi, const float* A, const float* W, const float* b,
-                        const float* R, const float* vec, float* C, int N, int K,
-                        hipStream_t stream)
+                        const float* R, float* C, int N, int K, hipStream_t stream)
 {
   dim3 g((N+63)/64, NI/64), blk(256);
   switch(epi){
-    case 0: gemm_k<0><<<g,blk,0,stream>>>(A,W,b,R,vec,C,N,K); break;
-    case 1: gemm_k<1><<<g,blk,0,stream>>>(A,W,b,R,vec,C,N,K); break;
-    case 2: gemm_k<2><<<g,blk,0,stream>>>(A,W,b,R,vec,C,N,K); break;
-    case 3: gemm_k<3><<<g,blk,0,stream>>>(A,W,b,R,vec,C,N,K); break;
-    case 4: gemm_k<4><<<g,blk,0,stream>>>(A,W,b,R,vec,C,N,K); break;
-    case 5: gemm_k<5><<<g,blk,0,stream>>>(A,W,b,R,vec,C,N,K); break;
+    case 0: gemm_k<0><<<g,blk,0,stream>>>(A,W,b,R,C,N,K); break;
+    case 1: gemm_k<1><<<g,blk,0,stream>>>(A,W,b,R,C,N,K); break;
+    case 2: gemm_k<2><<<g,blk,0,stream>>>(A,W,b,R,C,N,K); break;
+    case 3: gemm_k<3><<<g,blk,0,stream>>>(A,W,b,R,C,N,K); break;
   }
 }
 
@@ -792,18 +868,12 @@
   float* q2        = WS((size_t)NI*DIM);
   float* wsumb     = WS((size_t)NI*DIM);
   float* wv_hist   = WS((size_t)NSTEPS_*NI*DIM);
-  float* wg        = WS((size_t)NI*NMEM_);
-  float* mem_sc    = WS((size_t)NI*NMEM_);
   float* a_state   = WS((size_t)NI*NMEM_);
   float* c_state   = WS((size_t)NI*NMEM_*NSTEPS_);
-  float* h48       = WS((size_t)NI*48);
   float* rbuf      = WS((size_t)NI*DIM);
   float* vbuf      = WS((size_t)NI*DIM);
   float* coll_ctx  = WS((size_t)NI*DIM);
   float* ver_ctx   = WS((size_t)NI*DIM);
-  float* sub60     = WS((size_t)NI*60);
-  float* gate5     = WS((size_t)NI*5);
-  float* budget5   = WS((size_t)NI*5);
   float* sparse    = WS((size_t)NI*NEXPERT_);
   float* base10    = WS((size_t)NI*ODIM);
   float* reflect10 = WS((size_t)NI*ODIM);
@@ -833,69 +903,55 @@
   unsigned short* vcw1b  = BS((size_t)2*1536*DIM);
   unsigned short* vcw2b  = BS((size_t)2*DIM*1536);
   unsigned short* upb    = bb + boff;
-  size_t upb_n = ((size_t)NEXPERT_*MAXE + 3072 + 4096) * DIM;
+  size_t upb_n = (size_t)TOTCOL*DIM;
   size_t base_bytes = off*sizeof(float) + boff*sizeof(unsigned short);
   bool use_upb = (ws_size >= base_bytes + upb_n*sizeof(unsigned short));
   unsigned short* hb = (unsigned short*)hbig;
-
-  auto thin = [&](const float* A1, int K1, const float* A2, int K2,
-                  const float* Wp, const float* bp, float* Cp, int NO, int post){
-    int total = NI*NO;
-    thin_k<<<(total+255)/256, 256, 0, stream>>>(A1,K1,A2,K2,Wp,bp,Cp,NO,post);
-  };
 
   launch_cvt(rf_w1, rfw1b, (size_t)3*1280*DIM, stream);
   launch_cvt(rf_w2, rfw2b, (size_t)3*DIM*1280, stream);
   launch_cvt(vc_w1, vcw1b, (size_t)2*1536*DIM, stream);
   launch_cvt(vc_w2, vcw2b, (size_t)2*DIM*1536, stream);
-  if (use_upb){
-    launch_cvt(exp_up,      upb,                                    (size_t)NEXPERT_*MAXE*DIM, stream);
-    launch_cvt(shared_up_w, upb + (size_t)NEXPERT_*MAXE*DIM,        (size_t)3072*DIM, stream);
-    launch_cvt(aux_up_w,    upb + (size_t)NEXPERT_*MAXE*DIM + (size_t)3072*DIM, (size_t)4096*DIM, stream);
-  }
+  if (use_upb)
+    cvtup_k<<<TOTCOL/64, 512, 0, stream>>>(exp_up, shared_up_w, aux_up_w, (short*)upb);
 
   atb_k<<<(DIM*DIM+255)/256, 256, 0, stream>>>(depth_k_w, depth_q_w, PdT, DIM, DIM, DIM);
   atb_k<<<(DIM*DIM+255)/256, 256, 0, stream>>>(coll_k_w,  coll_q_w,  PcT, DIM, DIM, DIM);
   atb_k<<<(DIM*DIM+255)/256, 256, 0, stream>>>(ver_k_w,   ver_q_w,   PvT, DIM, DIM, DIM);
   ab_k <<<(NMEM_*DIM+255)/256, 256, 0, stream>>>(mem_keys, mem_q_w, MK, NMEM_, DIM, DIM);
 
-  thin(x, DIM, nullptr, 0, Wm, bvec, base10, ODIM, 0);
-
   const float* cur = x;
   for (int s = 0; s < NSTEPS_; s++){
-    thin(cur, DIM, nullptr, 0, MK, nullptr, mem_sc, NMEM_, 2);
-    memread_k<<<NI/4, 256, 0, stream>>>(mem_sc, a_state, c_state, mem_vals, wv_hist, mem_read, s);
-    thin(cur, DIM, mem_read, DIM, mem_wg_w, mem_wg_b, wg, NMEM_, 1);
-    launch_gemm(1, cur, mem_wv_w, mem_wv_b, nullptr, nullptr,
+    memread2_k<<<NI/4, 256, 0, stream>>>(cur, MK, a_state, c_state, mem_vals,
+                                         wv_hist, mem_read, s);
+    memwrite_k<<<NI/4, 256, 0, stream>>>(cur, mem_read, mem_wg_w, mem_wg_b,
+                                         a_state, c_state, s);
+    launch_gemm(1, cur, mem_wv_w, mem_wv_b, nullptr,
                 wv_hist + (size_t)s*NI*DIM, DIM, DIM, stream);
-    state_k<<<(NI*NMEM_+255)/256, 256, 0, stream>>>(wg, a_state, c_state, s);
     if (s > 0){
-      launch_gemm(0, cur, PdT, nullptr, nullptr, nullptr, q2, DIM, DIM, stream);
+      launch_gemm(0, cur, PdT, nullptr, nullptr, q2, DIM, DIM, stream);
       bankattn_k<<<NI/4, 256, 0, stream>>>(q2, bank, wsumb, s);
-      launch_gemm(0, wsumb, depth_v_w, nullptr, nullptr, nullptr, depth_ctx, DIM, DIM, stream);
+      launch_gemm(0, wsumb, depth_v_w, nullptr, nullptr, depth_ctx, DIM, DIM, stream);
     }
     ln3_k<<<NI/4, 256, 0, stream>>>(cur, mem_read, (s > 0 ? depth_ctx : nullptr),
                                     rc_ln_s + (size_t)s*DIM, rc_ln_b + (size_t)s*DIM,
                                     cur_in, t_ln, nullptr);
     launch_gemm(2, t_ln, rc_w1 + (size_t)s*896*DIM, rc_b1 + (size_t)s*896,
-                nullptr, nullptr, hbig, 896, DIM, stream);
+                nullptr, hbig, 896, DIM, stream);
     launch_gemm(3, hbig, rc_w2 + (size_t)s*DIM*896, rc_b2 + (size_t)s*DIM,
-                cur_in, nullptr, cur_in, DIM, 896, stream);
-    launch_gemm(4, cur_in, ssm_in_w, nullptr, nullptr, ssm_decay, h48, 48, DIM, stream);
+                cur_in, cur_in, DIM, 896, stream);
     float* newcur = bank + (size_t)s*NI*DIM;
-    launch_gemm(5, h48, ssm_out_w, nullptr, cur_in, nullptr, newcur, DIM, 48, stream);
-    halt_k<<<NI/4, 256, 0, stream>>>(newcur, mem_read, depth_ctx, halt_w, halt_b,
-                                     mem_out_w, depth_out_w, mem_logits, depth_logits,
-                                     cum_halt, s);
+    ssmhalt_k<<<NI/4, 256, 0, stream>>>(cur_in, mem_read, depth_ctx,
+                                        ssm_in_w, ssm_out_w, ssm_decay,
+                                        halt_w, halt_b, mem_out_w, depth_out_w,
+                                        newcur, mem_logits, depth_logits, cum_halt, s);
     cur = newcur;
   }
 
-  thin(cur, DIM, nullptr, 0, sub_w, sub_b, sub60, 60, 0);
-  thin(cur, DIM, nullptr, 0, gate_w, gate_b, gate5, 5, 0);
-  thin(cur, DIM, nullptr, 0, budget_w, budget_b, budget5, 5, 0);
-  router_k<<<(NI+255)/256, 256, 0, stream>>>(sub60, gate5, budget5, sparse);
-
-  moe_k<<<dim3(NI/128, NEXPERT_+2), 512, 0, stream>>>(
+  router2_k<<<NI/4, 256, 0, stream>>>(cur, sub_w, sub_b, gate_w, gate_b,
+                                      budget_w, budget_b, sparse);
+
+  moe2_k<<<dim3(NI/128, 182), 512, 0, stream>>>(
       cur, x, exp_up, shared_up_w, aux_up_w, use_upb ? (const short*)upb : nullptr,
       exp_down, shared_down_w, aux_down_w, expert_pre, shared_pre, aux_pre);
 
@@ -927,18 +983,18 @@
     vsrc = vbuf;
   }
 
-  launch_gemm(0, cur, PcT, nullptr, nullptr, nullptr, q2, DIM, DIM, stream);
+  launch_gemm(0, cur, PcT, nullptr, nullptr, q2, DIM, DIM, stream);
   bankattn_k<<<NI/4, 256, 0, stream>>>(q2, bank, wsumb, NSTEPS_);
-  launch_gemm(0, wsumb, coll_v_w, nullptr, nullptr, nullptr, coll_ctx, DIM, DIM, stream);
-
-  launch_gemm(0, vbuf, PvT, nullptr, nullptr, nullptr, q2, DIM, DIM, stream);
+  launch_gemm(0, wsumb, coll_v_w, nullptr, nullptr, coll_ctx, DIM, DIM, stream);
+
+  launch_gemm(0, vbuf, PvT, nullptr, nullptr, q2, DIM, DIM, stream);
   bankattn_k<<<NI/4, 256, 0, stream>>>(q2, bank, wsumb, NSTEPS_);
-  launch_gemm(0, wsumb, ver_v_w, nullptr, nullptr, nullptr, ver_ctx, DIM, DIM, stream);
-
-  thin(rbuf,     DIM, nullptr, 0, reflect_out_w,    nullptr, reflect10, ODIM, 0);
-  thin(coll_ctx, DIM, nullptr, 0, coll_out_w,       nullptr, coll10,    ODIM, 0);
-  thin(ver_ctx,  DIM, nullptr, 0, ver_out_w,        nullptr, ver10,     ODIM, 0);
-  thin(vbuf,     DIM, nullptr, 0, correction_out_w, nullptr, corr10,    ODIM, 0);
+  launch_gemm(0, wsumb, ver_v_w, nullptr, nullptr, ver_ctx, DIM, DIM, stream);
+
+  heads_k<<<(NI*50 + 255)/256, 256, 0, stream>>>(
+      rbuf, coll_ctx, ver_ctx, vbuf, x,
+      reflect_out_w, coll_out_w, ver_out_w, correction_out_w, Wm, bvec,
+      reflect10, coll10, ver10, corr10, base10);
 
   final_k<<<(NI+255)/256, 256, 0, stream>>>(
       x, cur, vbuf, coll_ctx, ver_ctx,
```

Result: slower. 3.360 ms (+10.4%).
